# Performance work log

Hardware: AMD Instinct MI355X
Metric: run time of the kernel (lower is better)

The kernel has to match this reference:

```python
import jax, jax.numpy as jnp
import numpy as np

B, L, D, NLAYERS, MAX_NODES, DEG = 32, 512, 768, 3, 128, 8


def _build_graph():
    rng = np.random.default_rng(0)
    per = rng.integers(-32, 33, size=B // 2)
    sizes = np.concatenate([96 + per, 96 - per]).astype(np.int64)  # sum = 96*B = 3072, each in [64,128]
    N = int(sizes.sum())
    offs = np.concatenate([[0], np.cumsum(sizes)])
    batch = np.repeat(np.arange(B), sizes).astype(np.int64)
    pad_idx = np.zeros((B, MAX_NODES), np.int64)
    pad_mask = np.zeros((B, MAX_NODES), bool)
    src, dst = [], []
    for b in range(B):
        n = int(sizes[b])
        pad_idx[b, :n] = np.arange(offs[b], offs[b] + n)
        pad_mask[b, :n] = True
        src.append(rng.integers(offs[b], offs[b] + n, n * DEG))
        dst.append(rng.integers(offs[b], offs[b] + n, n * DEG))
    return N, batch, pad_idx, pad_mask, np.concatenate(src), np.concatenate(dst)


def setup_inputs() -> dict:
    N, batch, pad_idx, pad_mask, esrc, edst = _build_graph()
    key = jax.random.key(0)
    ks = jax.random.split(key, 8)
    s = 1.0 / np.sqrt(D)
    return {
        "x": jax.random.normal(ks[0], (N, D), jnp.float32),
        "text": jax.random.normal(ks[1], (B, L, D), jnp.float32),
        "batch_ent1_d_mask": jnp.ones((B, 1), jnp.float32),
        "batch_ent1_g_mask": jnp.ones((B, 1), jnp.float32),
        "gnn_ws": jax.random.normal(ks[2], (NLAYERS, D, D), jnp.float32) * s,
        "gnn_wn": jax.random.normal(ks[3], (NLAYERS, D, D), jnp.float32) * s,
        "gnn_b": jnp.zeros((NLAYERS, D), jnp.float32),
        "atom_w": jax.random.normal(ks[4], (D, D), jnp.float32) * s,
        "atom_b": jnp.zeros((D,), jnp.float32),
        "rand_emb": jax.random.normal(ks[5], (1, D), jnp.float32),
        "batch": jnp.asarray(batch),
        "pad_idx": jnp.asarray(pad_idx),
        "pad_mask": jnp.asarray(pad_mask),
        "edge_src": jnp.asarray(esrc),
        "edge_dst": jnp.asarray(edst),
    }


def reference(x, text, batch_ent1_d_mask, batch_ent1_g_mask, gnn_ws, gnn_wn, gnn_b,
              atom_w, atom_b, rand_emb, batch, pad_idx, pad_mask, edge_src, edge_dst):
    N = x.shape[0]
    E = edge_src.shape[0]
    maskf = pad_mask.astype(x.dtype)            # [B, M]
    n_per = maskf.sum(axis=1)                   # [B] num real nodes per graph
    # edge-neighbor mean counts (constants w.r.t. x)
    cnt = jax.ops.segment_sum(jnp.ones((E,), x.dtype), edge_dst, num_segments=N)
    inv_cnt = 1.0 / jnp.maximum(cnt, 1.0)
    cms = []
    for i in range(NLAYERS):
        # MoleGraphConv stand-in: mean neighbor aggregation + self transform
        msg = jax.ops.segment_sum(x[edge_src], edge_dst, num_segments=N) * inv_cnt[:, None]
        x = jax.nn.relu(x @ gnn_ws[i] + msg @ gnn_wn[i] + gnn_b[i])
        # ragged gather into padded [B, M, D]
        xp = x[pad_idx] * maskf[..., None]
        # graph -> text cross attention (softmax over text tokens; no mask needed)
        g2t = jax.nn.softmax(jnp.einsum('bmd,bld->bml', xp, text), axis=-1)
        g2t_out = jnp.einsum('bml,bld->bmd', g2t, text)            # [B, M, D]
        # text -> graph cross attention (mask padded nodes)
        t2g_logits = jnp.einsum('bld,bmd->blm', text, xp)
        t2g_logits = jnp.where(pad_mask[:, None, :], t2g_logits, jnp.float32(-1e9))
        t2g = jax.nn.softmax(t2g_logits, axis=-1)
        t2g_out = jnp.einsum('blm,bmd->bld', t2g, xp)              # [B, L, D]
        # mean over concatenated rows [n_i + L] per graph (pool_type=2)
        pooled = ((g2t_out * maskf[..., None]).sum(axis=1) + t2g_out.sum(axis=1)) \
                 / (n_per + jnp.float32(L))[:, None]
        cms.append(pooled)
    out_cms = jnp.mean(jnp.stack(cms, axis=1), axis=1)              # mean over layers
    out_t = text[:, 0, :]
    # scatter-mean of final node features per graph
    gsum = jax.ops.segment_sum(x, batch, num_segments=B)
    gcnt = jax.ops.segment_sum(jnp.ones((N,), x.dtype), batch, num_segments=B)
    xg = gsum / jnp.maximum(gcnt, 1.0)[:, None]
    # dropout is a no-op in eval mode
    out_g = jnp.tanh(xg @ atom_w + atom_b)
    z = rand_emb[0]
    dg = batch_ent1_d_mask * batch_ent1_g_mask
    return jnp.concatenate([
        out_t * batch_ent1_d_mask + (1 - batch_ent1_d_mask) * z,
        out_g * batch_ent1_g_mask + (1 - batch_ent1_g_mask) * z,
        out_cms * dg + (1 - dg) * z,
    ], axis=-1)
```

## Files before the change

kernel.cpp:

```cpp
#include <hip/hip_runtime.h>

#define D 768
#define B 32
#define L 512
#define M 128
#define NNODES 3072
#define NEDGES 24576

using bf16x8 = __attribute__((ext_vector_type(8))) short;
using f32x4  = __attribute__((ext_vector_type(4))) float;

__device__ __forceinline__ float bf2f(unsigned short u) {
  union { unsigned int i; float f; } v; v.i = ((unsigned int)u) << 16; return v.f;
}
__device__ __forceinline__ unsigned short f2bf(float f) {
  union { float f; unsigned int i; } v; v.f = f;
  unsigned int x = v.i;
  return (unsigned short)((x + 0x7FFFu + ((x >> 16) & 1u)) >> 16);
}
__device__ __forceinline__ float ldf(const void* p, size_t i, int f32) {
  return f32 ? ((const float*)p)[i] : bf2f(((const unsigned short*)p)[i]);
}
__device__ __forceinline__ int ldi(const void* p, size_t i, int w64) {
  return w64 ? (int)((const long long*)p)[i] : ((const int*)p)[i];
}
__device__ __forceinline__ f32x4 mfma16(bf16x8 a, bf16x8 b, f32x4 c) {
  return __builtin_amdgcn_mfma_f32_16x16x32_bf16(a, b, c, 0, 0, 0);
}
__device__ __forceinline__ void gl_lds(const unsigned short* gsrc, unsigned short* lbase,
                                       int lane) {
  __builtin_amdgcn_global_load_lds(
      (const __attribute__((address_space(1))) unsigned int*)(gsrc + lane * 8),
      (__attribute__((address_space(3))) unsigned int*)lbase, 16, 0, 0);
}

__device__ __forceinline__ float pk_read(const unsigned short* P, int p, int l, int d) {
  return bf2f(P[(((size_t)(p * 24 + (d >> 5))) << 9) + ((((d & 31) >> 3) << 4) + l) * 8 + (d & 7)]);
}


__global__ void k_init(int* cnt, int* cursor, int* gcnt, float* pooled, float* xgacc,
                       const unsigned short* __restrict__ t,
                       const unsigned int* __restrict__ e, int* __restrict__ flags) {
  int i = blockIdx.x * 256 + threadIdx.x;
  if (i < NNODES) { cnt[i] = 0; cursor[i] = 0; }
  if (i < B) gcnt[i] = 0;
  if (i < B * D) { pooled[i] = 0.f; xgacc[i] = 0.f; }
  if (blockIdx.x == 0) {
    __shared__ int r0[256];
    __shared__ unsigned r1[256];
    int tid = threadIdx.x;
    int bad = 0;
    for (int j = tid; j < 8192; j += 256) {
      unsigned short u = t[2 * j];
      unsigned ex = (u >> 7) & 0xFF;
      if (ex >= 0xC0) bad = 1;
    }
    unsigned o = 0;
    for (int j = tid; j < NEDGES / 2; j += 256) o |= e[2 * j + 1];
    r0[tid] = bad; r1[tid] = o;
    __syncthreads();
    for (int s = 128; s > 0; s >>= 1) {
      if (tid < s) { r0[tid] |= r0[tid + s]; r1[tid] |= r1[tid + s]; }
      __syncthreads();
    }
    if (tid == 0) { flags[0] = r0[0]; flags[1] = (r1[0] == 0) ? 1 : 0; }
  }
}

__global__ __launch_bounds__(256) void k_pack_in(
    const void* __restrict__ x_in, unsigned short* __restrict__ x0,
    unsigned short* __restrict__ PkA, const void* __restrict__ text,
    unsigned short* __restrict__ Tpk, const int* __restrict__ flags) {
  __shared__ unsigned short buf[12288];
  int f = flags[0];
  int bid = blockIdx.x, tid = threadIdx.x;
  const void* src; unsigned short* dst; unsigned short* rows; int p;
  if (bid < NNODES / 16) { src = x_in; dst = PkA; rows = x0; p = bid; }
  else                   { src = text; dst = Tpk; rows = nullptr; p = bid - NNODES / 16; }
#pragma unroll
  for (int j = 0; j < 6; ++j) {
    int idx = j * 256 + tid;
    int r = idx / 96, c = idx % 96;
    size_t sbase = (size_t)(p * 16 + r) * 768 + c * 8;
    union { unsigned short v[8]; uint4 q; } u;
    if (f) {
      const float* sp = (const float*)src + sbase;
#pragma unroll
      for (int e = 0; e < 8; ++e) u.v[e] = f2bf(sp[e]);
    } else {
      const unsigned short* sp = (const unsigned short*)src + sbase;
#pragma unroll
      for (int e = 0; e < 8; ++e) u.v[e] = sp[e];
    }
    if (rows) *(uint4*)&rows[sbase] = u.q;
    int lpos = (c >> 2) * 64 + (c & 3) * 16 + r;
#pragma unroll
    for (int e = 0; e < 8; ++e) buf[lpos * 8 + e] = u.v[e];
  }
  __syncthreads();
  uint4* d4 = (uint4*)(dst + (size_t)p * 12288);
  const uint4* b4 = (const uint4*)buf;
#pragma unroll
  for (int j = 0; j < 6; ++j) d4[j * 256 + tid] = b4[j * 256 + tid];
}

__global__ __launch_bounds__(256) void k_pack(const unsigned short* __restrict__ src,
                                              unsigned short* __restrict__ dst) {
  __shared__ unsigned short buf[12288];
  int p = blockIdx.x, tid = threadIdx.x;
#pragma unroll
  for (int j = 0; j < 6; ++j) {
    int idx = j * 256 + tid;
    int r = idx / 96, c = idx % 96;
    size_t sbase = (size_t)(p * 16 + r) * 768 + c * 8;
    uint4 q = *(const uint4*)(src + sbase);
    int lpos = (c >> 2) * 64 + (c & 3) * 16 + r;
    *(uint4*)&buf[lpos * 8] = q;
  }
  __syncthreads();
  uint4* d4 = (uint4*)(dst + (size_t)p * 12288);
  const uint4* b4 = (const uint4*)buf;
#pragma unroll
  for (int j = 0; j < 6; ++j) d4[j * 256 + tid] = b4[j * 256 + tid];
}

__global__ __launch_bounds__(256) void k_wpack(
    const void* __restrict__ Ws, const void* __restrict__ Wn, const void* __restrict__ Aw,
    const int* __restrict__ flags, unsigned short* __restrict__ WsPk,
    unsigned short* __restrict__ WnPk, unsigned short* __restrict__ AwPk) {
  __shared__ unsigned short buf[2048];
  int f = flags[0];
  int z = blockIdx.z;
  const void* src; unsigned short* dst; size_t zoff;
  if (z < 3)      { src = Ws; zoff = (size_t)z * D * D;       dst = WsPk + zoff; }
  else if (z < 6) { src = Wn; zoff = (size_t)(z - 3) * D * D; dst = WnPk + zoff; }
  else            { src = Aw; zoff = 0;                       dst = AwPk; }
  int n0 = blockIdx.x * 64, kk = blockIdx.y;
  int tid = threadIdx.x;
  int kl = tid >> 3, c8 = tid & 7;
  size_t sbase = zoff + (size_t)(kk * 32 + kl) * D + n0 + c8 * 8;
  unsigned short v[8];
  if (f) {
    const float* sp = (const float*)src + sbase;
#pragma unroll
    for (int e = 0; e < 8; ++e) v[e] = f2bf(sp[e]);
  } else {
    const unsigned short* sp = (const unsigned short*)src + sbase;
#pragma unroll
    for (int e = 0; e < 8; ++e) v[e] = sp[e];
  }
  int ebit = kl & 7, quad = kl >> 3;
#pragma unroll
  for (int i = 0; i < 8; ++i) {
    int nl = c8 * 8 + i;
    int pl = nl >> 4;
    int lane = quad * 16 + (nl & 15);
    buf[pl * 512 + lane * 8 + ebit] = v[i];
  }
  __syncthreads();
  int pl = tid >> 6, pos = tid & 63;
  int pG = blockIdx.x * 4 + pl;
  uint4 q = *(const uint4*)&buf[pl * 512 + pos * 8];
  *(uint4*)&dst[(((size_t)(pG * 24 + kk)) << 9) + pos * 8] = q;
}

__global__ void k_count(const void* __restrict__ edst, const void* __restrict__ batch,
                        const int* __restrict__ flags, int* __restrict__ cnt,
                        int* __restrict__ gcnt) {
  int w = flags[1];
  int i = blockIdx.x * 256 + threadIdx.x;
  if (i < NEDGES) atomicAdd(&cnt[ldi(edst, i, w)], 1);
  if (i < NNODES) atomicAdd(&gcnt[ldi(batch, i, w)], 1);
}

__global__ void k_scan(const int* __restrict__ cnt, int* __restrict__ rowstart) {
  __shared__ int a[NNODES], b[NNODES];
  int tid = threadIdx.x;
  for (int i = tid; i < NNODES; i += 1024) a[i] = cnt[i];
  __syncthreads();
  int* s = a; int* d = b;
  for (int off = 1; off < NNODES; off <<= 1) {
    for (int i = tid; i < NNODES; i += 1024)
      d[i] = s[i] + (i >= off ? s[i - off] : 0);
    __syncthreads();
    int* t = s; s = d; d = t;
  }
  for (int i = tid; i < NNODES; i += 1024) rowstart[i + 1] = s[i];
  if (tid == 0) rowstart[0] = 0;
}

__global__ void k_scatter(const void* __restrict__ esrc, const void* __restrict__ edst,
                          const int* __restrict__ flags, const int* __restrict__ rowstart,
                          int* __restrict__ cursor, int* __restrict__ csr) {
  int w = flags[1];
  int i = blockIdx.x * 256 + threadIdx.x;
  if (i < NEDGES) {
    int dd = ldi(edst, i, w);
    int pos = atomicAdd(&cursor[dd], 1);
    csr[rowstart[dd] + pos] = ldi(esrc, i, w);
  }
}


__global__ __launch_bounds__(256) void k_msg_pack(
    const unsigned short* __restrict__ x, const int* __restrict__ cnt,
    const int* __restrict__ rowstart, const int* __restrict__ csr,
    unsigned short* __restrict__ Mpk) {
  __shared__ unsigned short buf[12288];
  int p = blockIdx.x, tid = threadIdx.x;
  int w = tid >> 6, lane = tid & 63;
#pragma unroll
  for (int i = 0; i < 4; ++i) {
    int r = w * 4 + i;
    int n = p * 16 + r;
    int deg = cnt[n], base = rowstart[n];
    float inv = 1.0f / (float)(deg > 1 ? deg : 1);
    float a[12];
#pragma unroll
    for (int j = 0; j < 12; ++j) a[j] = 0.f;
    for (int e = 0; e < deg; ++e) {
      const uint2* xr = (const uint2*)(x + (size_t)csr[base + e] * D);
#pragma unroll
      for (int j = 0; j < 3; ++j) {
        uint2 v = xr[lane + j * 64];
        a[j * 4 + 0] += bf2f((unsigned short)(v.x & 0xFFFFu));
        a[j * 4 + 1] += bf2f((unsigned short)(v.x >> 16));
        a[j * 4 + 2] += bf2f((unsigned short)(v.y & 0xFFFFu));
        a[j * 4 + 3] += bf2f((unsigned short)(v.y >> 16));
      }
    }
#pragma unroll
    for (int j = 0; j < 3; ++j) {
      int d0 = (lane + j * 64) * 4;
      int c = d0 >> 3, e0 = d0 & 7;
      int lpos = (c >> 2) * 64 + (c & 3) * 16 + r;
      unsigned short* bp = &buf[lpos * 8 + e0];
      bp[0] = f2bf(a[j * 4 + 0] * inv);
      bp[1] = f2bf(a[j * 4 + 1] * inv);
      bp[2] = f2bf(a[j * 4 + 2] * inv);
      bp[3] = f2bf(a[j * 4 + 3] * inv);
    }
  }
  __syncthreads();
  uint4* d4 = (uint4*)(Mpk + (size_t)p * 12288);
  const uint4* b4 = (const uint4*)buf;
#pragma unroll
  for (int j = 0; j < 6; ++j) d4[j * 256 + tid] = b4[j * 256 + tid];
}

__global__ __launch_bounds__(256) void k_gemm_gnn(
    const unsigned short* __restrict__ Xpk, const unsigned short* __restrict__ Mpk,
    const unsigned short* __restrict__ WsPk, const unsigned short* __restrict__ WnPk,
    const void* __restrict__ bias, size_t bias_off, const int* __restrict__ flags,
    unsigned short* __restrict__ Y) {
  __shared__ __align__(16) unsigned short lds[6 * 4096];
  int f = flags[0];
  int tid = threadIdx.x;
  int wave = tid >> 6, lane = tid & 63;
  int q = lane >> 4, t = lane & 15;
  int wm = wave >> 1, wn = wave & 1;
  int pa = blockIdx.x * 4, pb = blockIdx.y * 4;
  f32x4 acc[2][2];
#pragma unroll
  for (int mi = 0; mi < 2; ++mi)
#pragma unroll
    for (int ni = 0; ni < 2; ++ni)
      acc[mi][ni] = (f32x4){0.f, 0.f, 0.f, 0.f};

  int c0 = wave * 2;
  int pan0A = (wave < 2) ? (pa + c0) : (pb + c0 - 4);
  for (int r = 0; r < 8; ++r) {
    int h = r >> 2;
    int kk0 = r * 6 - h * 24;
    const unsigned short* P = (wave < 2) ? (h ? Mpk : Xpk) : (h ? WnPk : WsPk);
#pragma unroll
    for (int st = 0; st < 6; ++st) {
      gl_lds(P + (((size_t)(pan0A * 24 + kk0 + st)) << 9), &lds[st * 4096 + c0 * 512], lane);
      gl_lds(P + (((size_t)((pan0A + 1) * 24 + kk0 + st)) << 9), &lds[st * 4096 + (c0 + 1) * 512], lane);
    }
    __syncthreads();
#pragma unroll
    for (int st = 0; st < 6; ++st) {
      bf16x8 a0 = *(const bf16x8*)&lds[st * 4096 + (wm * 2 + 0) * 512 + lane * 8];
      bf16x8 a1 = *(const bf16x8*)&lds[st * 4096 + (wm * 2 + 1) * 512 + lane * 8];
      bf16x8 b0 = *(const bf16x8*)&lds[st * 4096 + (4 + wn * 2 + 0) * 512 + lane * 8];
      bf16x8 b1 = *(const bf16x8*)&lds[st * 4096 + (4 + wn * 2 + 1) * 512 + lane * 8];
      acc[0][0] = mfma16(a0, b0, acc[0][0]);
      acc[0][1] = mfma16(a0, b1, acc[0][1]);
      acc[1][0] = mfma16(a1, b0, acc[1][0]);
      acc[1][1] = mfma16(a1, b1, acc[1][1]);
    }
    __syncthreads();
  }

#pragma unroll
  for (int ni = 0; ni < 2; ++ni) {
    int col = blockIdx.y * 64 + wn * 32 + ni * 16 + t;
    float bv = ldf(bias, bias_off + col, f);
#pragma unroll
    for (int mi = 0; mi < 2; ++mi) {
#pragma unroll
      for (int r = 0; r < 4; ++r) {
        int row = blockIdx.x * 64 + wm * 32 + mi * 16 + q * 4 + r;
        float v = acc[mi][ni][r] + bv;
        Y[(size_t)row * D + col] = f2bf(v > 0.f ? v : 0.f);
      }
    }
  }
}

__global__ __launch_bounds__(256) void k_xp_pack(
    const unsigned short* __restrict__ Xn, const void* __restrict__ pidx,
    const int* __restrict__ flags, const int* __restrict__ gcnt,
    unsigned short* __restrict__ xp, unsigned short* __restrict__ XpPk,
    float* __restrict__ xgacc) {
  __shared__ unsigned short rows[16 * 776];
  int p = blockIdx.x, tid = threadIdx.x;
  int w64 = flags[1];
  int r = tid >> 4, c16 = tid & 15;
  int bm = p * 16 + r;
  int b = bm >> 7, m = bm & 127;
  int nb = gcnt[b];
  uint4* dl = (uint4*)&rows[r * 776];
  if (m < nb) {
    const uint4* srcr = (const uint4*)(Xn + (size_t)ldi(pidx, bm, w64) * D);
#pragma unroll
    for (int j = 0; j < 6; ++j) dl[c16 + j * 16] = srcr[c16 + j * 16];
  } else {
    uint4 z = {0u, 0u, 0u, 0u};
#pragma unroll
    for (int j = 0; j < 6; ++j) dl[c16 + j * 16] = z;
  }
  __syncthreads();
#pragma unroll
  for (int j = 0; j < 6; ++j) {
    int idx = j * 256 + tid;
    int rr = idx / 96, cc = idx % 96;
    uint4 vv = *(const uint4*)&rows[rr * 776 + cc * 8];
    *(uint4*)&xp[(size_t)(p * 16 + rr) * D + cc * 8] = vv;
  }
  unsigned short* pb = XpPk + (size_t)p * 12288;
#pragma unroll
  for (int j = 0; j < 6; ++j) {
    int odx = j * 256 + tid;
    int kk = odx >> 6, lanep = odx & 63;
    int rr = lanep & 15, cg = lanep >> 4;
    int cc = kk * 4 + cg;
    uint4 vv = *(const uint4*)&rows[rr * 776 + cc * 8];
    *(uint4*)&pb[odx * 8] = vv;
  }
  if (xgacc) {
    int bb = p >> 3;
#pragma unroll
    for (int j = 0; j < 3; ++j) {
      int d = j * 256 + tid;
      float s = 0.f;
#pragma unroll
      for (int rr = 0; rr < 16; ++rr) s += bf2f(rows[rr * 776 + d]);
      atomicAdd(&xgacc[(size_t)bb * D + d], s);
    }
  }
}

__global__ __launch_bounds__(256) void k_scores(
    const unsigned short* __restrict__ XpPk, const unsigned short* __restrict__ Tpk,
    float* __restrict__ S) {
  __shared__ __align__(16) unsigned short lds[6 * 4096];
  int b = blockIdx.z;
  int tid = threadIdx.x;
  int wave = tid >> 6, lane = tid & 63;
  int q = lane >> 4, t = lane & 15;
  int wm = wave >> 1, wn = wave & 1;
  int pa = b * 8 + blockIdx.x * 4;
  int pb = b * 32 + blockIdx.y * 4;
  f32x4 acc[2][2];
#pragma unroll
  for (int mi = 0; mi < 2; ++mi)
#pragma unroll
    for (int ni = 0; ni < 2; ++ni)
      acc[mi][ni] = (f32x4){0.f, 0.f, 0.f, 0.f};

  int c0 = wave * 2;
  const unsigned short* P = (wave < 2) ? XpPk : Tpk;
  int pan0 = (wave < 2) ? (pa + c0) : (pb + c0 - 4);
  for (int r = 0; r < 4; ++r) {
    int kk0 = r * 6;
#pragma unroll
    for (int st = 0; st < 6; ++st) {
      gl_lds(P + (((size_t)(pan0 * 24 + kk0 + st)) << 9), &lds[st * 4096 + c0 * 512], lane);
      gl_lds(P + (((size_t)((pan0 + 1) * 24 + kk0 + st)) << 9), &lds[st * 4096 + (c0 + 1) * 512], lane);
    }
    __syncthreads();
#pragma unroll
    for (int st = 0; st < 6; ++st) {
      bf16x8 a0 = *(const bf16x8*)&lds[st * 4096 + (wm * 2 + 0) * 512 + lane * 8];
      bf16x8 a1 = *(const bf16x8*)&lds[st * 4096 + (wm * 2 + 1) * 512 + lane * 8];
      bf16x8 b0 = *(const bf16x8*)&lds[st * 4096 + (4 + wn * 2 + 0) * 512 + lane * 8];
      bf16x8 b1 = *(const bf16x8*)&lds[st * 4096 + (4 + wn * 2 + 1) * 512 + lane * 8];
      acc[0][0] = mfma16(a0, b0, acc[0][0]);
      acc[0][1] = mfma16(a0, b1, acc[0][1]);
      acc[1][0] = mfma16(a1, b0, acc[1][0]);
      acc[1][1] = mfma16(a1, b1, acc[1][1]);
    }
    __syncthreads();
  }

  float* Sb = S + (size_t)b * M * L;
#pragma unroll
  for (int ni = 0; ni < 2; ++ni) {
    int col = blockIdx.y * 64 + wn * 32 + ni * 16 + t;
#pragma unroll
    for (int mi = 0; mi < 2; ++mi) {
#pragma unroll
      for (int r = 0; r < 4; ++r) {
        int row = blockIdx.x * 64 + wm * 32 + mi * 16 + q * 4 + r;
        Sb[(size_t)row * L + col] = acc[mi][ni][r];
      }
    }
  }
}

__global__ __launch_bounds__(256) void k_stats(
    const float* __restrict__ S, const int* __restrict__ gcnt,
    float* __restrict__ rmax, float* __restrict__ rsum,
    float* __restrict__ cmaxv, float* __restrict__ csumv) {
  int bid = blockIdx.x, tid = threadIdx.x;
  if (bid < B * M) {
    __shared__ float red[4];
    int lane = tid & 63, wv = tid >> 6;
    const float* r = S + (size_t)bid * L;
    float s0 = r[tid], s1 = r[tid + 256];
    float m = fmaxf(s0, s1);
#pragma unroll
    for (int o = 32; o > 0; o >>= 1) m = fmaxf(m, __shfl_down(m, o));
    if (lane == 0) red[wv] = m;
    __syncthreads();
    float bm = fmaxf(fmaxf(red[0], red[1]), fmaxf(red[2], red[3]));
    __syncthreads();
    float e = __expf(s0 - bm) + __expf(s1 - bm);
#pragma unroll
    for (int o = 32; o > 0; o >>= 1) e += __shfl_down(e, o);
    if (lane == 0) red[wv] = e;
    __syncthreads();
    if (tid == 0) { rmax[bid] = bm; rsum[bid] = red[0] + red[1] + red[2] + red[3]; }
  } else {
    __shared__ float pm[4][64], ps[4][64];
    int cid = bid - B * M;
    int b = cid >> 3, ly = cid & 7;
    int w = tid >> 6, lane = tid & 63;
    int l = ly * 64 + lane;
    int nb = gcnt[b];
    const float* Sb = S + (size_t)b * M * L;
    int m0 = w * 32, m1 = min(m0 + 32, nb);
    float cm = -1e30f, cs = 0.f;
    for (int m = m0; m < m1; ++m) {
      float s = Sb[(size_t)m * L + l];
      if (s > cm) { cs = cs * __expf(cm - s) + 1.f; cm = s; }
      else cs += __expf(s - cm);
    }
    pm[w][lane] = cm; ps[w][lane] = cs;
    __syncthreads();
    if (w == 0) {
      float CM = -1e30f;
#pragma unroll
      for (int j = 0; j < 4; ++j) CM = fmaxf(CM, pm[j][lane]);
      float CS = 0.f;
#pragma unroll
      for (int j = 0; j < 4; ++j) CS += ps[j][lane] * __expf(pm[j][lane] - CM);
      cmaxv[b * L + l] = CM; csumv[b * L + l] = CS;
    }
  }
}

__global__ __launch_bounds__(256) void k_cross(
    const float* __restrict__ S, const float* __restrict__ rmax,
    const float* __restrict__ rsum, const float* __restrict__ cmaxv,
    const float* __restrict__ csumv, const int* __restrict__ gcnt,
    float* __restrict__ wv, float* __restrict__ t2gcol) {
  int bid = blockIdx.x, tid = threadIdx.x;
  if (bid < 256) {
    __shared__ float rm[M], ri[M];
    __shared__ float pw[4][64];
    int b = bid >> 3, ly = bid & 7;
    int w = tid >> 6, lane = tid & 63;
    if (tid < M) { rm[tid] = rmax[b * M + tid]; ri[tid] = 1.f / rsum[b * M + tid]; }
    __syncthreads();
    int l = ly * 64 + lane;
    int nb = gcnt[b];
    const float* Sb = S + (size_t)b * M * L;
    int m0 = w * 32, m1 = min(m0 + 32, nb);
    float wp = 0.f;
    for (int m = m0; m < m1; ++m)
      wp += __expf(Sb[(size_t)m * L + l] - rm[m]) * ri[m];
    pw[w][lane] = wp;
    __syncthreads();
    if (w == 0)
      wv[b * L + l] = pw[0][lane] + pw[1][lane] + pw[2][lane] + pw[3][lane];
  } else {
    __shared__ float red[4];
    int bm = bid - 256;
    int b = bm >> 7, m = bm & 127;
    int lane = tid & 63, w = tid >> 6;
    int nb = gcnt[b];
    float acc = 0.f;
    if (m < nb) {
      const float* r = S + (size_t)bm * L;
      const float* cm = cmaxv + b * L;
      const float* cs = csumv + b * L;
      acc = __expf(r[tid] - cm[tid]) / cs[tid]
          + __expf(r[tid + 256] - cm[tid + 256]) / cs[tid + 256];
    }
#pragma unroll
    for (int o = 32; o > 0; o >>= 1) acc += __shfl_down(acc, o);
    if (lane == 0) red[w] = acc;
    __syncthreads();
    if (tid == 0) t2gcol[bm] = red[0] + red[1] + red[2] + red[3];
  }
}

__global__ __launch_bounds__(256) void k_pooled(
    const float* __restrict__ wv, const float* __restrict__ t2gcol,
    const unsigned short* __restrict__ Tpk, const unsigned short* __restrict__ xp,
    const int* __restrict__ gcnt, float* __restrict__ pooled) {
  int b = blockIdx.x;
  int d = blockIdx.y * 256 + threadIdx.x;
  int c = blockIdx.z;
  float acc = 0.f;
  if (c < 8) {
    int l0 = c * 64;
    for (int l = l0; l < l0 + 64; ++l) {
      int p = b * 32 + (l >> 4);
      acc += wv[b * L + l] * pk_read(Tpk, p, l & 15, d);
    }
  } else {
    const unsigned short* Xb = xp + (size_t)b * M * D;
    int mm0 = (c - 8) * 64;
    for (int m = mm0; m < mm0 + 64; ++m) acc += t2gcol[b * M + m] * bf2f(Xb[(size_t)m * D + d]);
  }
  atomicAdd(&pooled[(size_t)b * D + d], acc / ((float)gcnt[b] + 512.f));
}


__global__ __launch_bounds__(256) void k_atom(const float* __restrict__ xgacc,
                                              const int* __restrict__ gcnt,
                                              const unsigned short* __restrict__ AwPk,
                                              float* __restrict__ gpre) {
  int tid = threadIdx.x;
  int w = tid >> 6, lane = tid & 63;
  int q = lane >> 4, t = lane & 15;
  int nbase = blockIdx.x * 64 + w * 16;
  int pb = nbase >> 4;
  int n0 = gcnt[t], n1 = gcnt[16 + t];
  float inv0 = 1.f / (float)(n0 > 1 ? n0 : 1);
  float inv1 = 1.f / (float)(n1 > 1 ? n1 : 1);
  f32x4 acc[2];
  acc[0] = (f32x4){0.f, 0.f, 0.f, 0.f};
  acc[1] = (f32x4){0.f, 0.f, 0.f, 0.f};
  for (int kk = 0; kk < 24; ++kk) {
    const float* s0 = xgacc + (size_t)t * D + kk * 32 + q * 8;
    const float* s1 = xgacc + (size_t)(16 + t) * D + kk * 32 + q * 8;
    union { unsigned short v[8]; bf16x8 f; } a0, a1;
#pragma unroll
    for (int j = 0; j < 8; ++j) { a0.v[j] = f2bf(s0[j] * inv0); a1.v[j] = f2bf(s1[j] * inv1); }
    bf16x8 bv = *(const bf16x8*)(AwPk + (((size_t)(pb * 24 + kk)) << 9) + (lane << 3));
    acc[0] = mfma16(a0.f, bv, acc[0]);
    acc[1] = mfma16(a1.f, bv, acc[1]);
  }
#pragma unroll
  for (int mi = 0; mi < 2; ++mi)
#pragma unroll
    for (int r = 0; r < 4; ++r) {
      int row = mi * 16 + q * 4 + r;
      gpre[(size_t)row * D + nbase + t] = acc[mi][r];
    }
}

__global__ __launch_bounds__(256) void k_final(
    const unsigned short* __restrict__ Tpk, const float* __restrict__ gpre,
    const float* __restrict__ pooled, const void* __restrict__ ab,
    const void* __restrict__ dmask, const void* __restrict__ gmask,
    const void* __restrict__ remb, const int* __restrict__ flags,
    void* __restrict__ out) {
  int f = flags[0];
  int b = blockIdx.x, tid = threadIdx.x;
  float dm = ldf(dmask, b, f);
  float gm = ldf(gmask, b, f);
  float dg = dm * gm;
  size_t base = (size_t)b * 2304;
#pragma unroll
  for (int j = 0; j < 3; ++j) {
    int d = tid + j * 256;
    float z = ldf(remb, d, f);
    float tv = pk_read(Tpk, b * 32, 0, d);
    float o0 = tv * dm + (1.f - dm) * z;
    float gv = tanhf(gpre[(size_t)b * D + d] + ldf(ab, d, f));
    float o1 = gv * gm + (1.f - gm) * z;
    float p = pooled[(size_t)b * D + d] * (1.f / 3.f);
    float o2 = p * dg + (1.f - dg) * z;
    if (f) {
      float* of = (float*)out;
      of[base + d] = o0; of[base + 768 + d] = o1; of[base + 1536 + d] = o2;
    } else {
      unsigned short* ob = (unsigned short*)out;
      ob[base + d] = f2bf(o0); ob[base + 768 + d] = f2bf(o1); ob[base + 1536 + d] = f2bf(o2);
    }
  }
}

extern "C" void kernel_launch(void* const* d_in, const int* in_sizes, int n_in,
                              void* d_out, int out_size, void* d_ws, size_t ws_size,
                              hipStream_t stream) {
  const void* x_in  = d_in[0];
  const void* text  = d_in[1];
  const void* dmask = d_in[2];
  const void* gmask = d_in[3];
  const void* gws   = d_in[4];
  const void* gwn   = d_in[5];
  const void* gb    = d_in[6];
  const void* aw    = d_in[7];
  const void* ab    = d_in[8];
  const void* remb  = d_in[9];
  const void* batch = d_in[10];
  const void* pidx  = d_in[11];
  const void* esrc  = d_in[13];
  const void* edst  = d_in[14];

  char* wsp = (char*)d_ws;
  size_t off = 0;
  auto carve = [&](size_t bytes) -> void* {
    void* p = wsp + off;
    off += (bytes + 255) & ~(size_t)255;
    return p;
  };
  int* flags = (int*)carve(2 * 4);
  unsigned short* x0    = (unsigned short*)carve((size_t)NNODES * D * 2);
  unsigned short* xA    = (unsigned short*)carve((size_t)NNODES * D * 2);
  unsigned short* xB    = (unsigned short*)carve((size_t)NNODES * D * 2);
  unsigned short* PkA   = (unsigned short*)carve((size_t)NNODES * D * 2);
  unsigned short* PkB   = (unsigned short*)carve((size_t)NNODES * D * 2);
  unsigned short* Mpk   = (unsigned short*)carve((size_t)NNODES * D * 2);
  unsigned short* Tpk   = (unsigned short*)carve((size_t)B * L * D * 2);
  unsigned short* WsPk  = (unsigned short*)carve((size_t)3 * D * D * 2);
  unsigned short* WnPk  = (unsigned short*)carve((size_t)3 * D * D * 2);
  unsigned short* AwPk  = (unsigned short*)carve((size_t)D * D * 2);
  unsigned short* xp    = (unsigned short*)carve((size_t)B * M * D * 2);
  unsigned short* XpPk  = (unsigned short*)carve((size_t)B * M * D * 2);
  float* xgacc   = (float*)carve((size_t)B * D * 4);
  float* gpre    = (float*)carve((size_t)B * D * 4);
  float* S       = (float*)carve((size_t)B * M * L * 4);
  float* rmax    = (float*)carve((size_t)B * M * 4);
  float* rsum    = (float*)carve((size_t)B * M * 4);
  float* wv      = (float*)carve((size_t)B * L * 4);
  float* cmaxv   = (float*)carve((size_t)B * L * 4);
  float* csumv   = (float*)carve((size_t)B * L * 4);
  float* t2gcol  = (float*)carve((size_t)B * M * 4);
  float* pooled  = (float*)carve((size_t)B * D * 4);
  int* cnt      = (int*)carve((size_t)NNODES * 4);
  int* rowstart = (int*)carve((size_t)(NNODES + 1) * 4);
  int* cursor   = (int*)carve((size_t)NNODES * 4);
  int* gcnt     = (int*)carve((size_t)B * 4);
  int* csr      = (int*)carve((size_t)NEDGES * 4);

  k_init<<<96, 256, 0, stream>>>(cnt, cursor, gcnt, pooled, xgacc,
                                 (const unsigned short*)text, (const unsigned int*)edst, flags);
  k_pack_in<<<NNODES / 16 + B * L / 16, 256, 0, stream>>>(x_in, x0, PkA, text, Tpk, flags);
  k_wpack<<<dim3(12, 24, 7), 256, 0, stream>>>(gws, gwn, aw, flags, WsPk, WnPk, AwPk);
  k_count<<<96, 256, 0, stream>>>(edst, batch, flags, cnt, gcnt);
  k_scan<<<1, 1024, 0, stream>>>(cnt, rowstart);
  k_scatter<<<96, 256, 0, stream>>>(esrc, edst, flags, rowstart, cursor, csr);

  const unsigned short* xsrc = x0;
  const unsigned short* Apk = PkA;
  unsigned short* Y[3]   = {xA, xB, xA};
  unsigned short* Npk[3] = {PkB, PkA, nullptr};
  for (int i = 0; i < 3; ++i) {
    k_msg_pack<<<NNODES / 16, 256, 0, stream>>>(xsrc, cnt, rowstart, csr, Mpk);
    k_gemm_gnn<<<dim3(48, 12), 256, 0, stream>>>(Apk, Mpk, WsPk + (size_t)i * D * D,
                                                 WnPk + (size_t)i * D * D, gb, (size_t)i * D,
                                                 flags, Y[i]);
    if (i < 2) k_pack<<<NNODES / 16, 256, 0, stream>>>(Y[i], Npk[i]);
    k_xp_pack<<<B * M / 16, 256, 0, stream>>>(Y[i], pidx, flags, gcnt, xp, XpPk,
                                              (i == 2) ? xgacc : nullptr);
    k_scores<<<dim3(2, 8, B), 256, 0, stream>>>(XpPk, Tpk, S);
    k_stats<<<B * M + 256, 256, 0, stream>>>(S, gcnt, rmax, rsum, cmaxv, csumv);
    k_cross<<<256 + B * M, 256, 0, stream>>>(S, rmax, rsum, cmaxv, csumv, gcnt, wv, t2gcol);
    k_pooled<<<dim3(B, 3, 10), 256, 0, stream>>>(wv, t2gcol, Tpk, xp, gcnt, pooled);
    xsrc = Y[i];
    Apk = Npk[i];
  }
  k_atom<<<12, 256, 0, stream>>>(xgacc, gcnt, AwPk, gpre);
  k_final<<<B, 256, 0, stream>>>(Tpk, gpre, pooled, ab, dmask, gmask, remb, flags, d_out);
}
```

Baseline: 471.2 us.

## Fuse independent stages into combined launches and overlap GNN layers with attention

```diff
diff --git a/kernel.cpp b/kernel.cpp
--- a/kernel.cpp
+++ b/kernel.cpp
@@ -36,6 +36,448 @@
 
 __device__ __forceinline__ float pk_read(const unsigned short* P, int p, int l, int d) {
   return bf2f(P[(((size_t)(p * 24 + (d >> 5))) << 9) + ((((d & 31) >> 3) << 4) + l) * 8 + (d & 7)]);
+}
+
+
+__device__ void d_pack_in(const void* src, unsigned short* rows, unsigned short* dst,
+                          int p, int tid, int f, char* smem) {
+  unsigned short* buf = (unsigned short*)smem;
+#pragma unroll
+  for (int j = 0; j < 6; ++j) {
+    int idx = j * 256 + tid;
+    int r = idx / 96, c = idx % 96;
+    size_t sbase = (size_t)(p * 16 + r) * 768 + c * 8;
+    union { unsigned short v[8]; uint4 q; } u;
+    if (f) {
+      const float* sp = (const float*)src + sbase;
+#pragma unroll
+      for (int e = 0; e < 8; ++e) u.v[e] = f2bf(sp[e]);
+    } else {
+      const unsigned short* sp = (const unsigned short*)src + sbase;
+#pragma unroll
+      for (int e = 0; e < 8; ++e) u.v[e] = sp[e];
+    }
+    if (rows) *(uint4*)&rows[sbase] = u.q;
+    int lpos = (c >> 2) * 64 + (c & 3) * 16 + r;
+#pragma unroll
+    for (int e = 0; e < 8; ++e) buf[lpos * 8 + e] = u.v[e];
+  }
+  __syncthreads();
+  uint4* d4 = (uint4*)(dst + (size_t)p * 12288);
+  const uint4* b4 = (const uint4*)buf;
+#pragma unroll
+  for (int j = 0; j < 6; ++j) d4[j * 256 + tid] = b4[j * 256 + tid];
+}
+
+__device__ void d_pack(const unsigned short* src, unsigned short* dst,
+                       int p, int tid, char* smem) {
+  unsigned short* buf = (unsigned short*)smem;
+#pragma unroll
+  for (int j = 0; j < 6; ++j) {
+    int idx = j * 256 + tid;
+    int r = idx / 96, c = idx % 96;
+    size_t sbase = (size_t)(p * 16 + r) * 768 + c * 8;
+    uint4 q = *(const uint4*)(src + sbase);
+    int lpos = (c >> 2) * 64 + (c & 3) * 16 + r;
+    *(uint4*)&buf[lpos * 8] = q;
+  }
+  __syncthreads();
+  uint4* d4 = (uint4*)(dst + (size_t)p * 12288);
+  const uint4* b4 = (const uint4*)buf;
+#pragma unroll
+  for (int j = 0; j < 6; ++j) d4[j * 256 + tid] = b4[j * 256 + tid];
+}
+
+__device__ void d_wpack(const void* Ws, const void* Wn, const void* Aw, int f,
+                        unsigned short* WsPk, unsigned short* WnPk, unsigned short* AwPk,
+                        int r0, int tid, char* smem) {
+  unsigned short* buf = (unsigned short*)smem;
+  int z = r0 / 288, rem = r0 % 288;
+  int nblk = rem % 12, kk = rem / 12;
+  const void* src; unsigned short* dst; size_t zoff;
+  if (z < 3)      { src = Ws; zoff = (size_t)z * D * D;       dst = WsPk + zoff; }
+  else if (z < 6) { src = Wn; zoff = (size_t)(z - 3) * D * D; dst = WnPk + zoff; }
+  else            { src = Aw; zoff = 0;                       dst = AwPk; }
+  int n0 = nblk * 64;
+  int kl = tid >> 3, c8 = tid & 7;
+  size_t sbase = zoff + (size_t)(kk * 32 + kl) * D + n0 + c8 * 8;
+  unsigned short v[8];
+  if (f) {
+    const float* sp = (const float*)src + sbase;
+#pragma unroll
+    for (int e = 0; e < 8; ++e) v[e] = f2bf(sp[e]);
+  } else {
+    const unsigned short* sp = (const unsigned short*)src + sbase;
+#pragma unroll
+    for (int e = 0; e < 8; ++e) v[e] = sp[e];
+  }
+  int ebit = kl & 7, quad = kl >> 3;
+#pragma unroll
+  for (int i = 0; i < 8; ++i) {
+    int nl = c8 * 8 + i;
+    int pl = nl >> 4;
+    int lane = quad * 16 + (nl & 15);
+    buf[pl * 512 + lane * 8 + ebit] = v[i];
+  }
+  __syncthreads();
+  int pl = tid >> 6, pos = tid & 63;
+  int pG = nblk * 4 + pl;
+  uint4 q = *(const uint4*)&buf[pl * 512 + pos * 8];
+  *(uint4*)&dst[(((size_t)(pG * 24 + kk)) << 9) + pos * 8] = q;
+}
+
+__device__ void d_count(const void* edst, const void* batch, int w,
+                        int* cnt, int* gcnt, int i) {
+  if (i < NEDGES) atomicAdd(&cnt[ldi(edst, i, w)], 1);
+  if (i < NNODES) atomicAdd(&gcnt[ldi(batch, i, w)], 1);
+}
+
+__device__ void d_msg(const unsigned short* x, const int* cnt, const int* rowstart,
+                      const int* csr, unsigned short* Mpk, int p, int tid, char* smem) {
+  unsigned short* buf = (unsigned short*)smem;
+  int w = tid >> 6, lane = tid & 63;
+#pragma unroll
+  for (int i = 0; i < 4; ++i) {
+    int r = w * 4 + i;
+    int n = p * 16 + r;
+    int deg = cnt[n], base = rowstart[n];
+    float inv = 1.0f / (float)(deg > 1 ? deg : 1);
+    float a[12];
+#pragma unroll
+    for (int j = 0; j < 12; ++j) a[j] = 0.f;
+    for (int e = 0; e < deg; ++e) {
+      const uint2* xr = (const uint2*)(x + (size_t)csr[base + e] * D);
+#pragma unroll
+      for (int j = 0; j < 3; ++j) {
+        uint2 v = xr[lane + j * 64];
+        a[j * 4 + 0] += bf2f((unsigned short)(v.x & 0xFFFFu));
+        a[j * 4 + 1] += bf2f((unsigned short)(v.x >> 16));
+        a[j * 4 + 2] += bf2f((unsigned short)(v.y & 0xFFFFu));
+        a[j * 4 + 3] += bf2f((unsigned short)(v.y >> 16));
+      }
+    }
+#pragma unroll
+    for (int j = 0; j < 3; ++j) {
+      int d0 = (lane + j * 64) * 4;
+      int c = d0 >> 3, e0 = d0 & 7;
+      int lpos = (c >> 2) * 64 + (c & 3) * 16 + r;
+      unsigned short* bp = &buf[lpos * 8 + e0];
+      bp[0] = f2bf(a[j * 4 + 0] * inv);
+      bp[1] = f2bf(a[j * 4 + 1] * inv);
+      bp[2] = f2bf(a[j * 4 + 2] * inv);
+      bp[3] = f2bf(a[j * 4 + 3] * inv);
+    }
+  }
+  __syncthreads();
+  uint4* d4 = (uint4*)(Mpk + (size_t)p * 12288);
+  const uint4* b4 = (const uint4*)buf;
+#pragma unroll
+  for (int j = 0; j < 6; ++j) d4[j * 256 + tid] = b4[j * 256 + tid];
+}
+
+__device__ void d_gemm(const unsigned short* Xpk, const unsigned short* Mpk,
+                       const unsigned short* WsPk, const unsigned short* WnPk,
+                       const void* bias, size_t bias_off, int f,
+                       unsigned short* Y, int bx, int by, int tid, char* smem) {
+  unsigned short* lds = (unsigned short*)smem;
+  int wave = tid >> 6, lane = tid & 63;
+  int q = lane >> 4, t = lane & 15;
+  int wm = wave >> 1, wn = wave & 1;
+  int pa = bx * 4, pb = by * 4;
+  f32x4 acc[2][2];
+#pragma unroll
+  for (int mi = 0; mi < 2; ++mi)
+#pragma unroll
+    for (int ni = 0; ni < 2; ++ni)
+      acc[mi][ni] = (f32x4){0.f, 0.f, 0.f, 0.f};
+  int c0 = wave * 2;
+  int pan0 = (wave < 2) ? (pa + c0) : (pb + c0 - 4);
+  for (int r = 0; r < 8; ++r) {
+    int h = r >> 2;
+    int kk0 = r * 6 - h * 24;
+    const unsigned short* P = (wave < 2) ? (h ? Mpk : Xpk) : (h ? WnPk : WsPk);
+#pragma unroll
+    for (int st = 0; st < 6; ++st) {
+      gl_lds(P + (((size_t)(pan0 * 24 + kk0 + st)) << 9), &lds[st * 4096 + c0 * 512], lane);
+      gl_lds(P + (((size_t)((pan0 + 1) * 24 + kk0 + st)) << 9), &lds[st * 4096 + (c0 + 1) * 512], lane);
+    }
+    __syncthreads();
+#pragma unroll
+    for (int st = 0; st < 6; ++st) {
+      bf16x8 a0 = *(const bf16x8*)&lds[st * 4096 + (wm * 2 + 0) * 512 + lane * 8];
+      bf16x8 a1 = *(const bf16x8*)&lds[st * 4096 + (wm * 2 + 1) * 512 + lane * 8];
+      bf16x8 b0 = *(const bf16x8*)&lds[st * 4096 + (4 + wn * 2 + 0) * 512 + lane * 8];
+      bf16x8 b1 = *(const bf16x8*)&lds[st * 4096 + (4 + wn * 2 + 1) * 512 + lane * 8];
+      acc[0][0] = mfma16(a0, b0, acc[0][0]);
+      acc[0][1] = mfma16(a0, b1, acc[0][1]);
+      acc[1][0] = mfma16(a1, b0, acc[1][0]);
+      acc[1][1] = mfma16(a1, b1, acc[1][1]);
+    }
+    __syncthreads();
+  }
+#pragma unroll
+  for (int ni = 0; ni < 2; ++ni) {
+    int col = by * 64 + wn * 32 + ni * 16 + t;
+    float bv = ldf(bias, bias_off + col, f);
+#pragma unroll
+    for (int mi = 0; mi < 2; ++mi) {
+#pragma unroll
+      for (int r = 0; r < 4; ++r) {
+        int row = bx * 64 + wm * 32 + mi * 16 + q * 4 + r;
+        float v = acc[mi][ni][r] + bv;
+        Y[(size_t)row * D + col] = f2bf(v > 0.f ? v : 0.f);
+      }
+    }
+  }
+}
+
+__device__ void d_xp(const unsigned short* Xn, const void* pidx, int w64,
+                     const int* gcnt, unsigned short* xp, unsigned short* XpPk,
+                     float* xgacc, int p, int tid, char* smem) {
+  unsigned short* rows = (unsigned short*)smem;
+  int r = tid >> 4, c16 = tid & 15;
+  int bm = p * 16 + r;
+  int b = bm >> 7, m = bm & 127;
+  int nb = gcnt[b];
+  uint4* dl = (uint4*)&rows[r * 776];
+  if (m < nb) {
+    const uint4* srcr = (const uint4*)(Xn + (size_t)ldi(pidx, bm, w64) * D);
+#pragma unroll
+    for (int j = 0; j < 6; ++j) dl[c16 + j * 16] = srcr[c16 + j * 16];
+  } else {
+    uint4 z = {0u, 0u, 0u, 0u};
+#pragma unroll
+    for (int j = 0; j < 6; ++j) dl[c16 + j * 16] = z;
+  }
+  __syncthreads();
+#pragma unroll
+  for (int j = 0; j < 6; ++j) {
+    int idx = j * 256 + tid;
+    int rr = idx / 96, cc = idx % 96;
+    uint4 vv = *(const uint4*)&rows[rr * 776 + cc * 8];
+    *(uint4*)&xp[(size_t)(p * 16 + rr) * D + cc * 8] = vv;
+  }
+  unsigned short* pb = XpPk + (size_t)p * 12288;
+#pragma unroll
+  for (int j = 0; j < 6; ++j) {
+    int odx = j * 256 + tid;
+    int kk = odx >> 6, lanep = odx & 63;
+    int rr = lanep & 15, cg = lanep >> 4;
+    int cc = kk * 4 + cg;
+    uint4 vv = *(const uint4*)&rows[rr * 776 + cc * 8];
+    *(uint4*)&pb[odx * 8] = vv;
+  }
+  if (xgacc) {
+    int bb = p >> 3;
+#pragma unroll
+    for (int j = 0; j < 3; ++j) {
+      int d = j * 256 + tid;
+      float s = 0.f;
+#pragma unroll
+      for (int rr = 0; rr < 16; ++rr) s += bf2f(rows[rr * 776 + d]);
+      atomicAdd(&xgacc[(size_t)bb * D + d], s);
+    }
+  }
+}
+
+__device__ void d_scores(const unsigned short* XpPk, const unsigned short* Tpk,
+                         float* S, int bx, int by, int bz, int tid, char* smem) {
+  unsigned short* lds = (unsigned short*)smem;
+  int wave = tid >> 6, lane = tid & 63;
+  int q = lane >> 4, t = lane & 15;
+  int wm = wave >> 1, wn = wave & 1;
+  int pa = bz * 8 + bx * 4;
+  int pb = bz * 32 + by * 4;
+  f32x4 acc[2][2];
+#pragma unroll
+  for (int mi = 0; mi < 2; ++mi)
+#pragma unroll
+    for (int ni = 0; ni < 2; ++ni)
+      acc[mi][ni] = (f32x4){0.f, 0.f, 0.f, 0.f};
+  int c0 = wave * 2;
+  const unsigned short* P = (wave < 2) ? XpPk : Tpk;
+  int pan0 = (wave < 2) ? (pa + c0) : (pb + c0 - 4);
+  for (int r = 0; r < 4; ++r) {
+    int kk0 = r * 6;
+#pragma unroll
+    for (int st = 0; st < 6; ++st) {
+      gl_lds(P + (((size_t)(pan0 * 24 + kk0 + st)) << 9), &lds[st * 4096 + c0 * 512], lane);
+      gl_lds(P + (((size_t)((pan0 + 1) * 24 + kk0 + st)) << 9), &lds[st * 4096 + (c0 + 1) * 512], lane);
+    }
+    __syncthreads();
+#pragma unroll
+    for (int st = 0; st < 6; ++st) {
+      bf16x8 a0 = *(const bf16x8*)&lds[st * 4096 + (wm * 2 + 0) * 512 + lane * 8];
+      bf16x8 a1 = *(const bf16x8*)&lds[st * 4096 + (wm * 2 + 1) * 512 + lane * 8];
+      bf16x8 b0 = *(const bf16x8*)&lds[st * 4096 + (4 + wn * 2 + 0) * 512 + lane * 8];
+      bf16x8 b1 = *(const bf16x8*)&lds[st * 4096 + (4 + wn * 2 + 1) * 512 + lane * 8];
+      acc[0][0] = mfma16(a0, b0, acc[0][0]);
+      acc[0][1] = mfma16(a0, b1, acc[0][1]);
+      acc[1][0] = mfma16(a1, b0, acc[1][0]);
+      acc[1][1] = mfma16(a1, b1, acc[1][1]);
+    }
+    __syncthreads();
+  }
+  float* Sb = S + (size_t)bz * M * L;
+#pragma unroll
+  for (int ni = 0; ni < 2; ++ni) {
+    int col = by * 64 + wn * 32 + ni * 16 + t;
+#pragma unroll
+    for (int mi = 0; mi < 2; ++mi) {
+#pragma unroll
+      for (int r = 0; r < 4; ++r) {
+        int row = bx * 64 + wm * 32 + mi * 16 + q * 4 + r;
+        Sb[(size_t)row * L + col] = acc[mi][ni][r];
+      }
+    }
+  }
+}
+
+__device__ void d_stats(const float* S, const int* gcnt, float* rmax, float* rsum,
+                        float* cmaxv, float* csumv, int bid, int tid, char* smem) {
+  if (bid < B * M) {
+    float* red = (float*)smem;
+    int lane = tid & 63, wv = tid >> 6;
+    const float* r = S + (size_t)bid * L;
+    float s0 = r[tid], s1 = r[tid + 256];
+    float m = fmaxf(s0, s1);
+#pragma unroll
+    for (int o = 32; o > 0; o >>= 1) m = fmaxf(m, __shfl_down(m, o));
+    if (lane == 0) red[wv] = m;
+    __syncthreads();
+    float bm = fmaxf(fmaxf(red[0], red[1]), fmaxf(red[2], red[3]));
+    __syncthreads();
+    float e = __expf(s0 - bm) + __expf(s1 - bm);
+#pragma unroll
+    for (int o = 32; o > 0; o >>= 1) e += __shfl_down(e, o);
+    if (lane == 0) red[wv] = e;
+    __syncthreads();
+    if (tid == 0) { rmax[bid] = bm; rsum[bid] = red[0] + red[1] + red[2] + red[3]; }
+  } else {
+    float (*pm)[64] = (float(*)[64])smem;
+    float (*ps)[64] = (float(*)[64])(smem + 1024);
+    int cid = bid - B * M;
+    int b = cid >> 3, ly = cid & 7;
+    int w = tid >> 6, lane = tid & 63;
+    int l = ly * 64 + lane;
+    int nb = gcnt[b];
+    const float* Sb = S + (size_t)b * M * L;
+    int m0 = w * 32, m1 = min(m0 + 32, nb);
+    float cm = -1e30f, cs = 0.f;
+    for (int m = m0; m < m1; ++m) {
+      float s = Sb[(size_t)m * L + l];
+      if (s > cm) { cs = cs * __expf(cm - s) + 1.f; cm = s; }
+      else cs += __expf(s - cm);
+    }
+    pm[w][lane] = cm; ps[w][lane] = cs;
+    __syncthreads();
+    if (w == 0) {
+      float CM = -1e30f;
+#pragma unroll
+      for (int j = 0; j < 4; ++j) CM = fmaxf(CM, pm[j][lane]);
+      float CS = 0.f;
+#pragma unroll
+      for (int j = 0; j < 4; ++j) CS += ps[j][lane] * __expf(pm[j][lane] - CM);
+      cmaxv[b * L + l] = CM; csumv[b * L + l] = CS;
+    }
+  }
+}
+
+__device__ void d_cross(const float* S, const float* rmax, const float* rsum,
+                        const float* cmaxv, const float* csumv, const int* gcnt,
+                        float* wv, float* t2gcol, int bid, int tid, char* smem) {
+  if (bid < 256) {
+    float* rm = (float*)smem;
+    float* ri = (float*)(smem + 512);
+    float (*pw)[64] = (float(*)[64])(smem + 1024);
+    int b = bid >> 3, ly = bid & 7;
+    int w = tid >> 6, lane = tid & 63;
+    if (tid < M) { rm[tid] = rmax[b * M + tid]; ri[tid] = 1.f / rsum[b * M + tid]; }
+    __syncthreads();
+    int l = ly * 64 + lane;
+    int nb = gcnt[b];
+    const float* Sb = S + (size_t)b * M * L;
+    int m0 = w * 32, m1 = min(m0 + 32, nb);
+    float wp = 0.f;
+    for (int m = m0; m < m1; ++m)
+      wp += __expf(Sb[(size_t)m * L + l] - rm[m]) * ri[m];
+    pw[w][lane] = wp;
+    __syncthreads();
+    if (w == 0)
+      wv[b * L + l] = pw[0][lane] + pw[1][lane] + pw[2][lane] + pw[3][lane];
+  } else {
+    float* red = (float*)smem;
+    int bm = bid - 256;
+    int b = bm >> 7, m = bm & 127;
+    int lane = tid & 63, w = tid >> 6;
+    int nb = gcnt[b];
+    float acc = 0.f;
+    if (m < nb) {
+      const float* r = S + (size_t)bm * L;
+      const float* cm = cmaxv + b * L;
+      const float* cs = csumv + b * L;
+      acc = __expf(r[tid] - cm[tid]) / cs[tid]
+          + __expf(r[tid + 256] - cm[tid + 256]) / cs[tid + 256];
+    }
+#pragma unroll
+    for (int o = 32; o > 0; o >>= 1) acc += __shfl_down(acc, o);
+    if (lane == 0) red[w] = acc;
+    __syncthreads();
+    if (tid == 0) t2gcol[bm] = red[0] + red[1] + red[2] + red[3];
+  }
+}
+
+__device__ void d_pooled(const float* wv, const float* t2gcol, const unsigned short* Tpk,
+                         const unsigned short* xp, const int* gcnt, float* pooled,
+                         int bid, int tid) {
+  int b = bid & 31;
+  int rest = bid >> 5;
+  int y = rest % 3, c = rest / 3;
+  int d = y * 256 + tid;
+  float acc = 0.f;
+  if (c < 8) {
+    int l0 = c * 64;
+    for (int l = l0; l < l0 + 64; ++l) {
+      int p = b * 32 + (l >> 4);
+      acc += wv[b * L + l] * pk_read(Tpk, p, l & 15, d);
+    }
+  } else {
+    const unsigned short* Xb = xp + (size_t)b * M * D;
+    int mm0 = (c - 8) * 64;
+    for (int m = mm0; m < mm0 + 64; ++m) acc += t2gcol[b * M + m] * bf2f(Xb[(size_t)m * D + d]);
+  }
+  atomicAdd(&pooled[(size_t)b * D + d], acc / ((float)gcnt[b] + 512.f));
+}
+
+__device__ void d_atom(const float* xgacc, const int* gcnt, const unsigned short* AwPk,
+                       float* gpre, int bid, int tid) {
+  int w = tid >> 6, lane = tid & 63;
+  int q = lane >> 4, t = lane & 15;
+  int nbase = bid * 64 + w * 16;
+  int pb = nbase >> 4;
+  int n0 = gcnt[t], n1 = gcnt[16 + t];
+  float inv0 = 1.f / (float)(n0 > 1 ? n0 : 1);
+  float inv1 = 1.f / (float)(n1 > 1 ? n1 : 1);
+  f32x4 acc[2];
+  acc[0] = (f32x4){0.f, 0.f, 0.f, 0.f};
+  acc[1] = (f32x4){0.f, 0.f, 0.f, 0.f};
+  for (int kk = 0; kk < 24; ++kk) {
+    const float* s0 = xgacc + (size_t)t * D + kk * 32 + q * 8;
+    const float* s1 = xgacc + (size_t)(16 + t) * D + kk * 32 + q * 8;
+    union { unsigned short v[8]; bf16x8 f; } a0, a1;
+#pragma unroll
+    for (int j = 0; j < 8; ++j) { a0.v[j] = f2bf(s0[j] * inv0); a1.v[j] = f2bf(s1[j] * inv1); }
+    bf16x8 bv = *(const bf16x8*)(AwPk + (((size_t)(pb * 24 + kk)) << 9) + (lane << 3));
+    acc[0] = mfma16(a0.f, bv, acc[0]);
+    acc[1] = mfma16(a1.f, bv, acc[1]);
+  }
+#pragma unroll
+  for (int mi = 0; mi < 2; ++mi)
+#pragma unroll
+    for (int r = 0; r < 4; ++r) {
+      int row = mi * 16 + q * 4 + r;
+      gpre[(size_t)row * D + nbase + t] = acc[mi][r];
+    }
 }
 
 
@@ -68,110 +510,24 @@
   }
 }
 
-__global__ __launch_bounds__(256) void k_pack_in(
-    const void* __restrict__ x_in, unsigned short* __restrict__ x0,
-    unsigned short* __restrict__ PkA, const void* __restrict__ text,
-    unsigned short* __restrict__ Tpk, const int* __restrict__ flags) {
-  __shared__ unsigned short buf[12288];
-  int f = flags[0];
+__global__ __launch_bounds__(256) void k_setup2(
+    const void* x_in, unsigned short* x0, unsigned short* PkA,
+    const void* text, unsigned short* Tpk,
+    const void* Ws, const void* Wn, const void* Aw,
+    unsigned short* WsPk, unsigned short* WnPk, unsigned short* AwPk,
+    const void* edst, const void* batch, int* cnt, int* gcnt,
+    const int* __restrict__ flags) {
+  extern __shared__ char smem[];
   int bid = blockIdx.x, tid = threadIdx.x;
-  const void* src; unsigned short* dst; unsigned short* rows; int p;
-  if (bid < NNODES / 16) { src = x_in; dst = PkA; rows = x0; p = bid; }
-  else                   { src = text; dst = Tpk; rows = nullptr; p = bid - NNODES / 16; }
-#pragma unroll
-  for (int j = 0; j < 6; ++j) {
-    int idx = j * 256 + tid;
-    int r = idx / 96, c = idx % 96;
-    size_t sbase = (size_t)(p * 16 + r) * 768 + c * 8;
-    union { unsigned short v[8]; uint4 q; } u;
-    if (f) {
-      const float* sp = (const float*)src + sbase;
-#pragma unroll
-      for (int e = 0; e < 8; ++e) u.v[e] = f2bf(sp[e]);
-    } else {
-      const unsigned short* sp = (const unsigned short*)src + sbase;
-#pragma unroll
-      for (int e = 0; e < 8; ++e) u.v[e] = sp[e];
-    }
-    if (rows) *(uint4*)&rows[sbase] = u.q;
-    int lpos = (c >> 2) * 64 + (c & 3) * 16 + r;
-#pragma unroll
-    for (int e = 0; e < 8; ++e) buf[lpos * 8 + e] = u.v[e];
-  }
-  __syncthreads();
-  uint4* d4 = (uint4*)(dst + (size_t)p * 12288);
-  const uint4* b4 = (const uint4*)buf;
-#pragma unroll
-  for (int j = 0; j < 6; ++j) d4[j * 256 + tid] = b4[j * 256 + tid];
-}
-
-__global__ __launch_bounds__(256) void k_pack(const unsigned short* __restrict__ src,
-                                              unsigned short* __restrict__ dst) {
-  __shared__ unsigned short buf[12288];
-  int p = blockIdx.x, tid = threadIdx.x;
-#pragma unroll
-  for (int j = 0; j < 6; ++j) {
-    int idx = j * 256 + tid;
-    int r = idx / 96, c = idx % 96;
-    size_t sbase = (size_t)(p * 16 + r) * 768 + c * 8;
-    uint4 q = *(const uint4*)(src + sbase);
-    int lpos = (c >> 2) * 64 + (c & 3) * 16 + r;
-    *(uint4*)&buf[lpos * 8] = q;
-  }
-  __syncthreads();
-  uint4* d4 = (uint4*)(dst + (size_t)p * 12288);
-  const uint4* b4 = (const uint4*)buf;
-#pragma unroll
-  for (int j = 0; j < 6; ++j) d4[j * 256 + tid] = b4[j * 256 + tid];
-}
-
-__global__ __launch_bounds__(256) void k_wpack(
-    const void* __restrict__ Ws, const void* __restrict__ Wn, const void* __restrict__ Aw,
-    const int* __restrict__ flags, unsigned short* __restrict__ WsPk,
-    unsigned short* __restrict__ WnPk, unsigned short* __restrict__ AwPk) {
-  __shared__ unsigned short buf[2048];
-  int f = flags[0];
-  int z = blockIdx.z;
-  const void* src; unsigned short* dst; size_t zoff;
-  if (z < 3)      { src = Ws; zoff = (size_t)z * D * D;       dst = WsPk + zoff; }
-  else if (z < 6) { src = Wn; zoff = (size_t)(z - 3) * D * D; dst = WnPk + zoff; }
-  else            { src = Aw; zoff = 0;                       dst = AwPk; }
-  int n0 = blockIdx.x * 64, kk = blockIdx.y;
-  int tid = threadIdx.x;
-  int kl = tid >> 3, c8 = tid & 7;
-  size_t sbase = zoff + (size_t)(kk * 32 + kl) * D + n0 + c8 * 8;
-  unsigned short v[8];
-  if (f) {
-    const float* sp = (const float*)src + sbase;
-#pragma unroll
-    for (int e = 0; e < 8; ++e) v[e] = f2bf(sp[e]);
+  if (bid < 1216) {
+    int f = flags[0];
+    if (bid < NNODES / 16) d_pack_in(x_in, x0, PkA, bid, tid, f, smem);
+    else d_pack_in(text, nullptr, Tpk, bid - NNODES / 16, tid, f, smem);
+  } else if (bid < 3232) {
+    d_wpack(Ws, Wn, Aw, flags[0], WsPk, WnPk, AwPk, bid - 1216, tid, smem);
   } else {
-    const unsigned short* sp = (const unsigned short*)src + sbase;
-#pragma unroll
-    for (int e = 0; e < 8; ++e) v[e] = sp[e];
-  }
-  int ebit = kl & 7, quad = kl >> 3;
-#pragma unroll
-  for (int i = 0; i < 8; ++i) {
-    int nl = c8 * 8 + i;
-    int pl = nl >> 4;
-    int lane = quad * 16 + (nl & 15);
-    buf[pl * 512 + lane * 8 + ebit] = v[i];
-  }
-  __syncthreads();
-  int pl = tid >> 6, pos = tid & 63;
-  int pG = blockIdx.x * 4 + pl;
-  uint4 q = *(const uint4*)&buf[pl * 512 + pos * 8];
-  *(uint4*)&dst[(((size_t)(pG * 24 + kk)) << 9) + pos * 8] = q;
-}
-
-__global__ void k_count(const void* __restrict__ edst, const void* __restrict__ batch,
-                        const int* __restrict__ flags, int* __restrict__ cnt,
-                        int* __restrict__ gcnt) {
-  int w = flags[1];
-  int i = blockIdx.x * 256 + threadIdx.x;
-  if (i < NEDGES) atomicAdd(&cnt[ldi(edst, i, w)], 1);
-  if (i < NNODES) atomicAdd(&gcnt[ldi(batch, i, w)], 1);
+    d_count(edst, batch, flags[1], cnt, gcnt, (bid - 3232) * 256 + tid);
+  }
 }
 
 __global__ void k_scan(const int* __restrict__ cnt, int* __restrict__ rowstart) {
@@ -202,378 +558,88 @@
   }
 }
 
-
-__global__ __launch_bounds__(256) void k_msg_pack(
-    const unsigned short* __restrict__ x, const int* __restrict__ cnt,
-    const int* __restrict__ rowstart, const int* __restrict__ csr,
-    unsigned short* __restrict__ Mpk) {
-  __shared__ unsigned short buf[12288];
-  int p = blockIdx.x, tid = threadIdx.x;
-  int w = tid >> 6, lane = tid & 63;
-#pragma unroll
-  for (int i = 0; i < 4; ++i) {
-    int r = w * 4 + i;
-    int n = p * 16 + r;
-    int deg = cnt[n], base = rowstart[n];
-    float inv = 1.0f / (float)(deg > 1 ? deg : 1);
-    float a[12];
-#pragma unroll
-    for (int j = 0; j < 12; ++j) a[j] = 0.f;
-    for (int e = 0; e < deg; ++e) {
-      const uint2* xr = (const uint2*)(x + (size_t)csr[base + e] * D);
-#pragma unroll
-      for (int j = 0; j < 3; ++j) {
-        uint2 v = xr[lane + j * 64];
-        a[j * 4 + 0] += bf2f((unsigned short)(v.x & 0xFFFFu));
-        a[j * 4 + 1] += bf2f((unsigned short)(v.x >> 16));
-        a[j * 4 + 2] += bf2f((unsigned short)(v.y & 0xFFFFu));
-        a[j * 4 + 3] += bf2f((unsigned short)(v.y >> 16));
-      }
-    }
-#pragma unroll
-    for (int j = 0; j < 3; ++j) {
-      int d0 = (lane + j * 64) * 4;
-      int c = d0 >> 3, e0 = d0 & 7;
-      int lpos = (c >> 2) * 64 + (c & 3) * 16 + r;
-      unsigned short* bp = &buf[lpos * 8 + e0];
-      bp[0] = f2bf(a[j * 4 + 0] * inv);
-      bp[1] = f2bf(a[j * 4 + 1] * inv);
-      bp[2] = f2bf(a[j * 4 + 2] * inv);
-      bp[3] = f2bf(a[j * 4 + 3] * inv);
-    }
-  }
-  __syncthreads();
-  uint4* d4 = (uint4*)(Mpk + (size_t)p * 12288);
-  const uint4* b4 = (const uint4*)buf;
-#pragma unroll
-  for (int j = 0; j < 6; ++j) d4[j * 256 + tid] = b4[j * 256 + tid];
-}
-
-__global__ __launch_bounds__(256) void k_gemm_gnn(
-    const unsigned short* __restrict__ Xpk, const unsigned short* __restrict__ Mpk,
-    const unsigned short* __restrict__ WsPk, const unsigned short* __restrict__ WnPk,
-    const void* __restrict__ bias, size_t bias_off, const int* __restrict__ flags,
-    unsigned short* __restrict__ Y) {
-  __shared__ __align__(16) unsigned short lds[6 * 4096];
-  int f = flags[0];
-  int tid = threadIdx.x;
-  int wave = tid >> 6, lane = tid & 63;
-  int q = lane >> 4, t = lane & 15;
-  int wm = wave >> 1, wn = wave & 1;
-  int pa = blockIdx.x * 4, pb = blockIdx.y * 4;
-  f32x4 acc[2][2];
-#pragma unroll
-  for (int mi = 0; mi < 2; ++mi)
-#pragma unroll
-    for (int ni = 0; ni < 2; ++ni)
-      acc[mi][ni] = (f32x4){0.f, 0.f, 0.f, 0.f};
-
-  int c0 = wave * 2;
-  int pan0A = (wave < 2) ? (pa + c0) : (pb + c0 - 4);
-  for (int r = 0; r < 8; ++r) {
-    int h = r >> 2;
-    int kk0 = r * 6 - h * 24;
-    const unsigned short* P = (wave < 2) ? (h ? Mpk : Xpk) : (h ? WnPk : WsPk);
-#pragma unroll
-    for (int st = 0; st < 6; ++st) {
-      gl_lds(P + (((size_t)(pan0A * 24 + kk0 + st)) << 9), &lds[st * 4096 + c0 * 512], lane);
-      gl_lds(P + (((size_t)((pan0A + 1) * 24 + kk0 + st)) << 9), &lds[st * 4096 + (c0 + 1) * 512], lane);
-    }
-    __syncthreads();
-#pragma unroll
-    for (int st = 0; st < 6; ++st) {
-      bf16x8 a0 = *(const bf16x8*)&lds[st * 4096 + (wm * 2 + 0) * 512 + lane * 8];
-      bf16x8 a1 = *(const bf16x8*)&lds[st * 4096 + (wm * 2 + 1) * 512 + lane * 8];
-      bf16x8 b0 = *(const bf16x8*)&lds[st * 4096 + (4 + wn * 2 + 0) * 512 + lane * 8];
-      bf16x8 b1 = *(const bf16x8*)&lds[st * 4096 + (4 + wn * 2 + 1) * 512 + lane * 8];
-      acc[0][0] = mfma16(a0, b0, acc[0][0]);
-      acc[0][1] = mfma16(a0, b1, acc[0][1]);
-      acc[1][0] = mfma16(a1, b0, acc[1][0]);
-      acc[1][1] = mfma16(a1, b1, acc[1][1]);
-    }
-    __syncthreads();
-  }
-
-#pragma unroll
-  for (int ni = 0; ni < 2; ++ni) {
-    int col = blockIdx.y * 64 + wn * 32 + ni * 16 + t;
-    float bv = ldf(bias, bias_off + col, f);
-#pragma unroll
-    for (int mi = 0; mi < 2; ++mi) {
-#pragma unroll
-      for (int r = 0; r < 4; ++r) {
-        int row = blockIdx.x * 64 + wm * 32 + mi * 16 + q * 4 + r;
-        float v = acc[mi][ni][r] + bv;
-        Y[(size_t)row * D + col] = f2bf(v > 0.f ? v : 0.f);
-      }
-    }
-  }
-}
-
-__global__ __launch_bounds__(256) void k_xp_pack(
-    const unsigned short* __restrict__ Xn, const void* __restrict__ pidx,
-    const int* __restrict__ flags, const int* __restrict__ gcnt,
-    unsigned short* __restrict__ xp, unsigned short* __restrict__ XpPk,
-    float* __restrict__ xgacc) {
-  __shared__ unsigned short rows[16 * 776];
-  int p = blockIdx.x, tid = threadIdx.x;
-  int w64 = flags[1];
-  int r = tid >> 4, c16 = tid & 15;
-  int bm = p * 16 + r;
-  int b = bm >> 7, m = bm & 127;
-  int nb = gcnt[b];
-  uint4* dl = (uint4*)&rows[r * 776];
-  if (m < nb) {
-    const uint4* srcr = (const uint4*)(Xn + (size_t)ldi(pidx, bm, w64) * D);
-#pragma unroll
-    for (int j = 0; j < 6; ++j) dl[c16 + j * 16] = srcr[c16 + j * 16];
-  } else {
-    uint4 z = {0u, 0u, 0u, 0u};
-#pragma unroll
-    for (int j = 0; j < 6; ++j) dl[c16 + j * 16] = z;
-  }
-  __syncthreads();
-#pragma unroll
-  for (int j = 0; j < 6; ++j) {
-    int idx = j * 256 + tid;
-    int rr = idx / 96, cc = idx % 96;
-    uint4 vv = *(const uint4*)&rows[rr * 776 + cc * 8];
-    *(uint4*)&xp[(size_t)(p * 16 + rr) * D + cc * 8] = vv;
-  }
-  unsigned short* pb = XpPk + (size_t)p * 12288;
-#pragma unroll
-  for (int j = 0; j < 6; ++j) {
-    int odx = j * 256 + tid;
-    int kk = odx >> 6, lanep = odx & 63;
-    int rr = lanep & 15, cg = lanep >> 4;
-    int cc = kk * 4 + cg;
-    uint4 vv = *(const uint4*)&rows[rr * 776 + cc * 8];
-    *(uint4*)&pb[odx * 8] = vv;
-  }
-  if (xgacc) {
-    int bb = p >> 3;
-#pragma unroll
-    for (int j = 0; j < 3; ++j) {
-      int d = j * 256 + tid;
-      float s = 0.f;
-#pragma unroll
-      for (int rr = 0; rr < 16; ++rr) s += bf2f(rows[rr * 776 + d]);
-      atomicAdd(&xgacc[(size_t)bb * D + d], s);
-    }
-  }
-}
-
-__global__ __launch_bounds__(256) void k_scores(
-    const unsigned short* __restrict__ XpPk, const unsigned short* __restrict__ Tpk,
-    float* __restrict__ S) {
-  __shared__ __align__(16) unsigned short lds[6 * 4096];
-  int b = blockIdx.z;
-  int tid = threadIdx.x;
-  int wave = tid >> 6, lane = tid & 63;
-  int q = lane >> 4, t = lane & 15;
-  int wm = wave >> 1, wn = wave & 1;
-  int pa = b * 8 + blockIdx.x * 4;
-  int pb = b * 32 + blockIdx.y * 4;
-  f32x4 acc[2][2];
-#pragma unroll
-  for (int mi = 0; mi < 2; ++mi)
-#pragma unroll
-    for (int ni = 0; ni < 2; ++ni)
-      acc[mi][ni] = (f32x4){0.f, 0.f, 0.f, 0.f};
-
-  int c0 = wave * 2;
-  const unsigned short* P = (wave < 2) ? XpPk : Tpk;
-  int pan0 = (wave < 2) ? (pa + c0) : (pb + c0 - 4);
-  for (int r = 0; r < 4; ++r) {
-    int kk0 = r * 6;
-#pragma unroll
-    for (int st = 0; st < 6; ++st) {
-      gl_lds(P + (((size_t)(pan0 * 24 + kk0 + st)) << 9), &lds[st * 4096 + c0 * 512], lane);
-      gl_lds(P + (((size_t)((pan0 + 1) * 24 + kk0 + st)) << 9), &lds[st * 4096 + (c0 + 1) * 512], lane);
-    }
-    __syncthreads();
-#pragma unroll
-    for (int st = 0; st < 6; ++st) {
-      bf16x8 a0 = *(const bf16x8*)&lds[st * 4096 + (wm * 2 + 0) * 512 + lane * 8];
-      bf16x8 a1 = *(const bf16x8*)&lds[st * 4096 + (wm * 2 + 1) * 512 + lane * 8];
-      bf16x8 b0 = *(const bf16x8*)&lds[st * 4096 + (4 + wn * 2 + 0) * 512 + lane * 8];
-      bf16x8 b1 = *(const bf16x8*)&lds[st * 4096 + (4 + wn * 2 + 1) * 512 + lane * 8];
-      acc[0][0] = mfma16(a0, b0, acc[0][0]);
-      acc[0][1] = mfma16(a0, b1, acc[0][1]);
-      acc[1][0] = mfma16(a1, b0, acc[1][0]);
-      acc[1][1] = mfma16(a1, b1, acc[1][1]);
-    }
-    __syncthreads();
-  }
-
-  float* Sb = S + (size_t)b * M * L;
-#pragma unroll
-  for (int ni = 0; ni < 2; ++ni) {
-    int col = blockIdx.y * 64 + wn * 32 + ni * 16 + t;
-#pragma unroll
-    for (int mi = 0; mi < 2; ++mi) {
-#pragma unroll
-      for (int r = 0; r < 4; ++r) {
-        int row = blockIdx.x * 64 + wm * 32 + mi * 16 + q * 4 + r;
-        Sb[(size_t)row * L + col] = acc[mi][ni][r];
-      }
-    }
-  }
-}
-
-__global__ __launch_bounds__(256) void k_stats(
-    const float* __restrict__ S, const int* __restrict__ gcnt,
-    float* __restrict__ rmax, float* __restrict__ rsum,
-    float* __restrict__ cmaxv, float* __restrict__ csumv) {
+__global__ __launch_bounds__(256) void k_msgp(
+    const unsigned short* x, const int* cnt, const int* rowstart, const int* csr,
+    unsigned short* Mpk) {
+  extern __shared__ char smem[];
+  d_msg(x, cnt, rowstart, csr, Mpk, blockIdx.x, threadIdx.x, smem);
+}
+
+__global__ __launch_bounds__(256) void k_gemm(
+    const unsigned short* Apk, const unsigned short* Mpk,
+    const unsigned short* WsPk, const unsigned short* WnPk,
+    const void* bias, unsigned long bias_off, const int* flags, unsigned short* Y) {
+  extern __shared__ char smem[];
+  int g = blockIdx.x;
+  d_gemm(Apk, Mpk, WsPk, WnPk, bias, bias_off, flags[0], Y, g % 48, g / 48,
+         threadIdx.x, smem);
+}
+
+__global__ __launch_bounds__(256) void k_postg(
+    const unsigned short* Y, unsigned short* Npk, int packN,
+    const void* pidx, const int* flags, const int* gcnt,
+    unsigned short* xp, unsigned short* XpPk, float* xgacc) {
+  extern __shared__ char smem[];
   int bid = blockIdx.x, tid = threadIdx.x;
-  if (bid < B * M) {
-    __shared__ float red[4];
-    int lane = tid & 63, wv = tid >> 6;
-    const float* r = S + (size_t)bid * L;
-    float s0 = r[tid], s1 = r[tid + 256];
-    float m = fmaxf(s0, s1);
-#pragma unroll
-    for (int o = 32; o > 0; o >>= 1) m = fmaxf(m, __shfl_down(m, o));
-    if (lane == 0) red[wv] = m;
-    __syncthreads();
-    float bm = fmaxf(fmaxf(red[0], red[1]), fmaxf(red[2], red[3]));
-    __syncthreads();
-    float e = __expf(s0 - bm) + __expf(s1 - bm);
-#pragma unroll
-    for (int o = 32; o > 0; o >>= 1) e += __shfl_down(e, o);
-    if (lane == 0) red[wv] = e;
-    __syncthreads();
-    if (tid == 0) { rmax[bid] = bm; rsum[bid] = red[0] + red[1] + red[2] + red[3]; }
-  } else {
-    __shared__ float pm[4][64], ps[4][64];
-    int cid = bid - B * M;
-    int b = cid >> 3, ly = cid & 7;
-    int w = tid >> 6, lane = tid & 63;
-    int l = ly * 64 + lane;
-    int nb = gcnt[b];
-    const float* Sb = S + (size_t)b * M * L;
-    int m0 = w * 32, m1 = min(m0 + 32, nb);
-    float cm = -1e30f, cs = 0.f;
-    for (int m = m0; m < m1; ++m) {
-      float s = Sb[(size_t)m * L + l];
-      if (s > cm) { cs = cs * __expf(cm - s) + 1.f; cm = s; }
-      else cs += __expf(s - cm);
-    }
-    pm[w][lane] = cm; ps[w][lane] = cs;
-    __syncthreads();
-    if (w == 0) {
-      float CM = -1e30f;
-#pragma unroll
-      for (int j = 0; j < 4; ++j) CM = fmaxf(CM, pm[j][lane]);
-      float CS = 0.f;
-#pragma unroll
-      for (int j = 0; j < 4; ++j) CS += ps[j][lane] * __expf(pm[j][lane] - CM);
-      cmaxv[b * L + l] = CM; csumv[b * L + l] = CS;
-    }
-  }
-}
-
-__global__ __launch_bounds__(256) void k_cross(
-    const float* __restrict__ S, const float* __restrict__ rmax,
-    const float* __restrict__ rsum, const float* __restrict__ cmaxv,
-    const float* __restrict__ csumv, const int* __restrict__ gcnt,
-    float* __restrict__ wv, float* __restrict__ t2gcol) {
+  if (bid < packN) d_pack(Y, Npk, bid, tid, smem);
+  else d_xp(Y, pidx, flags[1], gcnt, xp, XpPk, xgacc, bid - packN, tid, smem);
+}
+
+__global__ __launch_bounds__(256) void k_scmsg(
+    const unsigned short* XpPk, const unsigned short* Tpk, float* S,
+    int msgN, const unsigned short* x, const int* cnt, const int* rowstart,
+    const int* csr, unsigned short* Mpk) {
+  extern __shared__ char smem[];
   int bid = blockIdx.x, tid = threadIdx.x;
-  if (bid < 256) {
-    __shared__ float rm[M], ri[M];
-    __shared__ float pw[4][64];
-    int b = bid >> 3, ly = bid & 7;
-    int w = tid >> 6, lane = tid & 63;
-    if (tid < M) { rm[tid] = rmax[b * M + tid]; ri[tid] = 1.f / rsum[b * M + tid]; }
-    __syncthreads();
-    int l = ly * 64 + lane;
-    int nb = gcnt[b];
-    const float* Sb = S + (size_t)b * M * L;
-    int m0 = w * 32, m1 = min(m0 + 32, nb);
-    float wp = 0.f;
-    for (int m = m0; m < m1; ++m)
-      wp += __expf(Sb[(size_t)m * L + l] - rm[m]) * ri[m];
-    pw[w][lane] = wp;
-    __syncthreads();
-    if (w == 0)
-      wv[b * L + l] = pw[0][lane] + pw[1][lane] + pw[2][lane] + pw[3][lane];
-  } else {
-    __shared__ float red[4];
-    int bm = bid - 256;
-    int b = bm >> 7, m = bm & 127;
-    int lane = tid & 63, w = tid >> 6;
-    int nb = gcnt[b];
-    float acc = 0.f;
-    if (m < nb) {
-      const float* r = S + (size_t)bm * L;
-      const float* cm = cmaxv + b * L;
-      const float* cs = csumv + b * L;
-      acc = __expf(r[tid] - cm[tid]) / cs[tid]
-          + __expf(r[tid + 256] - cm[tid + 256]) / cs[tid + 256];
-    }
-#pragma unroll
-    for (int o = 32; o > 0; o >>= 1) acc += __shfl_down(acc, o);
-    if (lane == 0) red[w] = acc;
-    __syncthreads();
-    if (tid == 0) t2gcol[bm] = red[0] + red[1] + red[2] + red[3];
-  }
-}
-
-__global__ __launch_bounds__(256) void k_pooled(
-    const float* __restrict__ wv, const float* __restrict__ t2gcol,
-    const unsigned short* __restrict__ Tpk, const unsigned short* __restrict__ xp,
-    const int* __restrict__ gcnt, float* __restrict__ pooled) {
-  int b = blockIdx.x;
-  int d = blockIdx.y * 256 + threadIdx.x;
-  int c = blockIdx.z;
-  float acc = 0.f;
-  if (c < 8) {
-    int l0 = c * 64;
-    for (int l = l0; l < l0 + 64; ++l) {
-      int p = b * 32 + (l >> 4);
-      acc += wv[b * L + l] * pk_read(Tpk, p, l & 15, d);
-    }
-  } else {
-    const unsigned short* Xb = xp + (size_t)b * M * D;
-    int mm0 = (c - 8) * 64;
-    for (int m = mm0; m < mm0 + 64; ++m) acc += t2gcol[b * M + m] * bf2f(Xb[(size_t)m * D + d]);
-  }
-  atomicAdd(&pooled[(size_t)b * D + d], acc / ((float)gcnt[b] + 512.f));
-}
-
-
-__global__ __launch_bounds__(256) void k_atom(const float* __restrict__ xgacc,
-                                              const int* __restrict__ gcnt,
-                                              const unsigned short* __restrict__ AwPk,
-                                              float* __restrict__ gpre) {
-  int tid = threadIdx.x;
-  int w = tid >> 6, lane = tid & 63;
-  int q = lane >> 4, t = lane & 15;
-  int nbase = blockIdx.x * 64 + w * 16;
-  int pb = nbase >> 4;
-  int n0 = gcnt[t], n1 = gcnt[16 + t];
-  float inv0 = 1.f / (float)(n0 > 1 ? n0 : 1);
-  float inv1 = 1.f / (float)(n1 > 1 ? n1 : 1);
-  f32x4 acc[2];
-  acc[0] = (f32x4){0.f, 0.f, 0.f, 0.f};
-  acc[1] = (f32x4){0.f, 0.f, 0.f, 0.f};
-  for (int kk = 0; kk < 24; ++kk) {
-    const float* s0 = xgacc + (size_t)t * D + kk * 32 + q * 8;
-    const float* s1 = xgacc + (size_t)(16 + t) * D + kk * 32 + q * 8;
-    union { unsigned short v[8]; bf16x8 f; } a0, a1;
-#pragma unroll
-    for (int j = 0; j < 8; ++j) { a0.v[j] = f2bf(s0[j] * inv0); a1.v[j] = f2bf(s1[j] * inv1); }
-    bf16x8 bv = *(const bf16x8*)(AwPk + (((size_t)(pb * 24 + kk)) << 9) + (lane << 3));
-    acc[0] = mfma16(a0.f, bv, acc[0]);
-    acc[1] = mfma16(a1.f, bv, acc[1]);
-  }
-#pragma unroll
-  for (int mi = 0; mi < 2; ++mi)
-#pragma unroll
-    for (int r = 0; r < 4; ++r) {
-      int row = mi * 16 + q * 4 + r;
-      gpre[(size_t)row * D + nbase + t] = acc[mi][r];
-    }
+  if (bid < 512) d_scores(XpPk, Tpk, S, bid & 1, (bid >> 1) & 7, bid >> 4, tid, smem);
+  else d_msg(x, cnt, rowstart, csr, Mpk, bid - 512, tid, smem);
+}
+
+__global__ __launch_bounds__(256) void k_stgemm(
+    const float* S, const int* gcnt, float* rmax, float* rsum, float* cmaxv, float* csumv,
+    int gemmN, const unsigned short* Apk, const unsigned short* Mpk,
+    const unsigned short* WsPk, const unsigned short* WnPk,
+    const void* bias, unsigned long bias_off, const int* flags, unsigned short* Y) {
+  extern __shared__ char smem[];
+  int bid = blockIdx.x, tid = threadIdx.x;
+  if (bid < 4352) d_stats(S, gcnt, rmax, rsum, cmaxv, csumv, bid, tid, smem);
+  else {
+    int g = bid - 4352;
+    d_gemm(Apk, Mpk, WsPk, WnPk, bias, bias_off, flags[0], Y, g % 48, g / 48, tid, smem);
+  }
+}
+
+__global__ __launch_bounds__(256) void k_crpostg(
+    const float* S, const float* rmax, const float* rsum, const float* cmaxv,
+    const float* csumv, const int* gcnt, float* wv, float* t2gcol,
+    int packN, int xpN, const unsigned short* Y, unsigned short* Npk,
+    const void* pidx, const int* flags, unsigned short* xp, unsigned short* XpPk,
+    float* xgacc) {
+  extern __shared__ char smem[];
+  int bid = blockIdx.x, tid = threadIdx.x;
+  if (bid < 4352) d_cross(S, rmax, rsum, cmaxv, csumv, gcnt, wv, t2gcol, bid, tid, smem);
+  else {
+    int r = bid - 4352;
+    if (r < packN) d_pack(Y, Npk, r, tid, smem);
+    else d_xp(Y, pidx, flags[1], gcnt, xp, XpPk, xgacc, r - packN, tid, smem);
+  }
+}
+
+__global__ __launch_bounds__(256) void k_plscmsg(
+    const float* wv, const float* t2gcol, const unsigned short* Tpk,
+    const unsigned short* xpL, const int* gcnt, float* pooled,
+    int scN, const unsigned short* XpPk, float* S,
+    int msgN, const unsigned short* x, const int* cnt, const int* rowstart,
+    const int* csr, unsigned short* Mpk,
+    int atomN, const float* xgacc, const unsigned short* AwPk, float* gpre) {
+  extern __shared__ char smem[];
+  int bid = blockIdx.x, tid = threadIdx.x;
+  if (bid < 960) { d_pooled(wv, t2gcol, Tpk, xpL, gcnt, pooled, bid, tid); return; }
+  int r = bid - 960;
+  if (r < scN) { d_scores(XpPk, Tpk, S, r & 1, (r >> 1) & 7, r >> 4, tid, smem); return; }
+  r -= scN;
+  if (r < msgN) { d_msg(x, cnt, rowstart, csr, Mpk, r, tid, smem); return; }
+  d_atom(xgacc, gcnt, AwPk, gpre, r - msgN, tid);
 }
 
 __global__ __launch_bounds__(256) void k_final(
@@ -644,8 +710,10 @@
   unsigned short* WsPk  = (unsigned short*)carve((size_t)3 * D * D * 2);
   unsigned short* WnPk  = (unsigned short*)carve((size_t)3 * D * D * 2);
   unsigned short* AwPk  = (unsigned short*)carve((size_t)D * D * 2);
-  unsigned short* xp    = (unsigned short*)carve((size_t)B * M * D * 2);
-  unsigned short* XpPk  = (unsigned short*)carve((size_t)B * M * D * 2);
+  unsigned short* xpA   = (unsigned short*)carve((size_t)B * M * D * 2);
+  unsigned short* xpB   = (unsigned short*)carve((size_t)B * M * D * 2);
+  unsigned short* XpPkA = (unsigned short*)carve((size_t)B * M * D * 2);
+  unsigned short* XpPkB = (unsigned short*)carve((size_t)B * M * D * 2);
   float* xgacc   = (float*)carve((size_t)B * D * 4);
   float* gpre    = (float*)carve((size_t)B * D * 4);
   float* S       = (float*)carve((size_t)B * M * L * 4);
@@ -662,33 +730,42 @@
   int* gcnt     = (int*)carve((size_t)B * 4);
   int* csr      = (int*)carve((size_t)NEDGES * 4);
 
+  const size_t DD = (size_t)D * D;
+
   k_init<<<96, 256, 0, stream>>>(cnt, cursor, gcnt, pooled, xgacc,
                                  (const unsigned short*)text, (const unsigned int*)edst, flags);
-  k_pack_in<<<NNODES / 16 + B * L / 16, 256, 0, stream>>>(x_in, x0, PkA, text, Tpk, flags);
-  k_wpack<<<dim3(12, 24, 7), 256, 0, stream>>>(gws, gwn, aw, flags, WsPk, WnPk, AwPk);
-  k_count<<<96, 256, 0, stream>>>(edst, batch, flags, cnt, gcnt);
+  k_setup2<<<3328, 256, 24576, stream>>>(x_in, x0, PkA, text, Tpk, gws, gwn, aw,
+                                         WsPk, WnPk, AwPk, edst, batch, cnt, gcnt, flags);
   k_scan<<<1, 1024, 0, stream>>>(cnt, rowstart);
   k_scatter<<<96, 256, 0, stream>>>(esrc, edst, flags, rowstart, cursor, csr);
 
-  const unsigned short* xsrc = x0;
-  const unsigned short* Apk = PkA;
-  unsigned short* Y[3]   = {xA, xB, xA};
-  unsigned short* Npk[3] = {PkB, PkA, nullptr};
-  for (int i = 0; i < 3; ++i) {
-    k_msg_pack<<<NNODES / 16, 256, 0, stream>>>(xsrc, cnt, rowstart, csr, Mpk);
-    k_gemm_gnn<<<dim3(48, 12), 256, 0, stream>>>(Apk, Mpk, WsPk + (size_t)i * D * D,
-                                                 WnPk + (size_t)i * D * D, gb, (size_t)i * D,
-                                                 flags, Y[i]);
-    if (i < 2) k_pack<<<NNODES / 16, 256, 0, stream>>>(Y[i], Npk[i]);
-    k_xp_pack<<<B * M / 16, 256, 0, stream>>>(Y[i], pidx, flags, gcnt, xp, XpPk,
-                                              (i == 2) ? xgacc : nullptr);
-    k_scores<<<dim3(2, 8, B), 256, 0, stream>>>(XpPk, Tpk, S);
-    k_stats<<<B * M + 256, 256, 0, stream>>>(S, gcnt, rmax, rsum, cmaxv, csumv);
-    k_cross<<<256 + B * M, 256, 0, stream>>>(S, rmax, rsum, cmaxv, csumv, gcnt, wv, t2gcol);
-    k_pooled<<<dim3(B, 3, 10), 256, 0, stream>>>(wv, t2gcol, Tpk, xp, gcnt, pooled);
-    xsrc = Y[i];
-    Apk = Npk[i];
-  }
-  k_atom<<<12, 256, 0, stream>>>(xgacc, gcnt, AwPk, gpre);
-  k_final<<<B, 256, 0, stream>>>(Tpk, gpre, pooled, ab, dmask, gmask, remb, flags, d_out);
-}
+  k_msgp<<<192, 256, 24576, stream>>>(x0, cnt, rowstart, csr, Mpk);
+  k_gemm<<<576, 256, 49152, stream>>>(PkA, Mpk, WsPk, WnPk, gb, 0, flags, xA);
+  k_postg<<<448, 256, 24832, stream>>>(xA, PkB, 192, pidx, flags, gcnt, xpA, XpPkA, nullptr);
+  k_scmsg<<<704, 256, 49152, stream>>>(XpPkA, Tpk, S, 192, xA, cnt, rowstart, csr, Mpk);
+  k_stgemm<<<4928, 256, 49152, stream>>>(S, gcnt, rmax, rsum, cmaxv, csumv,
+                                         576, PkB, Mpk, WsPk + DD, WnPk + DD, gb, D, flags, xB);
+  k_crpostg<<<4800, 256, 24832, stream>>>(S, rmax, rsum, cmaxv, csumv, gcnt, wv, t2gcol,
+                                          192, 256, xB, PkA, pidx, flags, xpB, XpPkB, nullptr);
+  k_plscmsg<<<1664, 256, 49152, stream>>>(wv, t2gcol, Tpk, xpA, gcnt, pooled,
+                                          512, XpPkB, S, 192, xB, cnt, rowstart, csr, Mpk,
+                                          0, nullptr, nullptr, nullptr);
+  k_stgemm<<<4928, 256, 49152, stream>>>(S, gcnt, rmax, rsum, cmaxv, csumv,
+                                         576, PkA, Mpk, WsPk + 2 * DD, WnPk + 2 * DD,
+                                         gb, 2 * D, flags, xA);
+  k_crpostg<<<4608, 256, 24832, stream>>>(S, rmax, rsum, cmaxv, csumv, gcnt, wv, t2gcol,
+                                          0, 256, xA, nullptr, pidx, flags, xpA, XpPkA, xgacc);
+  k_plscmsg<<<1472, 256, 49152, stream>>>(wv, t2gcol, Tpk, xpB, gcnt, pooled,
+                                          512, XpPkA, S, 0, nullptr, nullptr, nullptr,
+                                          nullptr, nullptr, 0, nullptr, nullptr, nullptr);
+  k_stgemm<<<4352, 256, 2048, stream>>>(S, gcnt, rmax, rsum, cmaxv, csumv,
+                                        0, nullptr, nullptr, nullptr, nullptr,
+                                        nullptr, 0, flags, nullptr);
+  k_crpostg<<<4352, 256, 2048, stream>>>(S, rmax, rsum, cmaxv, csumv, gcnt, wv, t2gcol,
+                                         0, 0, nullptr, nullptr, pidx, flags,
+                                         nullptr, nullptr, nullptr);
+  k_plscmsg<<<972, 256, 2048, stream>>>(wv, t2gcol, Tpk, xpA, gcnt, pooled,
+                                        0, nullptr, nullptr, 0, nullptr, nullptr, nullptr,
+                                        nullptr, nullptr, 12, xgacc, AwPk, gpre);
+  k_final<<<32, 256, 0, stream>>>(Tpk, gpre, pooled, ab, dmask, gmask, remb, flags, d_out);
+}
```

Measured after the change: 454.6 us. -3.5%, faster.
